# Kernel tuning notes

Hardware: AMD Instinct MI355X
Metric: run time of the kernel (lower is better)

Reference implementation:

```python
import jax, jax.numpy as jnp
import numpy as np

D = 256          # d_model
NPRE = 16; NMLP = 16; NPOST = 16
K = 4            # top_k
P = NPRE * NMLP * NPOST   # 4096 pathways
HMAX = 5 * D     # max mlp expert hidden width (padded storage)
B, S = 8, 256


def _gelu(z):
    return jax.nn.gelu(z, approximate=False)  # torch nn.GELU default = exact erf


def _ln(z, g, b, eps=1e-5):
    mu = z.mean(-1, keepdims=True)
    v = ((z - mu) ** 2).mean(-1, keepdims=True)
    return (z - mu) * jax.lax.rsqrt(v + eps) * g + b


def setup_inputs() -> dict:
    key = jax.random.key(0)
    ks = jax.random.split(key, 8)

    def nrm(k, shape, scale):
        return jax.random.normal(k, shape, dtype=jnp.float32) * scale

    return {
        "x": nrm(ks[0], (B, S, D), 1.0),
        # router MLP (dropout inactive in eval)
        "rw1": nrm(ks[1], (D, 256), D ** -0.5), "rb1": jnp.zeros((256,), jnp.float32),
        "rw2": nrm(ks[2], (256, 128), 256 ** -0.5), "rb2": jnp.zeros((128,), jnp.float32),
        "rw3": nrm(ks[3], (128, P), 128 ** -0.5), "rb3": jnp.zeros((P,), jnp.float32),
        "temp": jnp.ones((1,), jnp.float32),
        # pre experts: Linear + LayerNorm + act
        "pw": nrm(ks[4], (NPRE, D, D), D ** -0.5), "pb": jnp.zeros((NPRE, D), jnp.float32),
        "pg": jnp.ones((NPRE, D), jnp.float32), "pbb": jnp.zeros((NPRE, D), jnp.float32),
        # mlp experts: variable hidden D*(2+i//4), padded to HMAX (unused cols sliced off)
        "mw1": nrm(ks[5], (NMLP, D, HMAX), D ** -0.5), "mb1": jnp.zeros((NMLP, HMAX), jnp.float32),
        "mw2": nrm(ks[6], (NMLP, HMAX, D), HMAX ** -0.5), "mb2": jnp.zeros((NMLP, D), jnp.float32),
        # post experts: Linear + (LayerNorm if even)
        "qw": nrm(ks[7], (NPOST, D, D), D ** -0.5), "qb": jnp.zeros((NPOST, D), jnp.float32),
        "qg": jnp.ones((NPOST, D), jnp.float32), "qbb": jnp.zeros((NPOST, D), jnp.float32),
    }


def reference(x, rw1, rb1, rw2, rb2, rw3, rb3, temp, pw, pb, pg, pbb,
              mw1, mb1, mw2, mb2, qw, qb, qg, qbb):
    Bv, Sv, Dv = x.shape
    N = Bv * Sv
    xt = x.reshape(N, Dv)

    # ---- router ----
    h = _gelu(xt @ rw1 + rb1)
    h = _gelu(h @ rw2 + rb2)
    scores = h @ rw3 + rb3                                  # [N, P]

    # ---- GLBL load-balance loss (softmax without temperature; torch.var unbiased) ----
    freq = jax.nn.softmax(scores, axis=-1).mean(0)          # [P]
    glbl_loss = P * jnp.var(freq, ddof=1)

    # ---- top-k pathway selection ----
    probs = jax.nn.softmax(scores / temp[0], axis=-1)
    top_vals, top_idx = jax.lax.top_k(probs, K)             # [N, K]
    pw_full = jnp.zeros((N, P), x.dtype).at[jnp.arange(N)[:, None], top_idx].set(top_vals)
    pathway_weights = pw_full / (pw_full.sum(-1, keepdims=True) + 1e-8)

    # ---- decompose pathway index -> (pre, mlp, post) ----
    pre_idx = top_idx // (NMLP * NPOST)
    rem = top_idx % (NMLP * NPOST)
    mlp_idx = rem // NPOST
    post_idx = rem % NPOST

    # ---- pre experts: compute all, gather per (token, slot) ----
    acts = [_gelu, jax.nn.relu, jnp.tanh]
    pre_all = jnp.stack(
        [acts[i % 3](_ln(xt @ pw[i] + pb[i], pg[i], pbb[i])) for i in range(NPRE)],
        axis=1)                                              # [N, NPRE, D]
    x_pre = jnp.take_along_axis(pre_all, pre_idx[:, :, None], axis=1)  # [N, K, D]

    # ---- mlp experts (variable hidden width), masked combine ----
    x_mlp = jnp.zeros_like(x_pre)
    for j in range(NMLP):
        hid = Dv * (2 + j // 4)
        a = _gelu if j % 2 == 0 else jax.nn.relu
        mid = a(jnp.einsum('nkd,dh->nkh', x_pre, mw1[j, :, :hid]) + mb1[j, :hid])
        out = jnp.einsum('nkh,hd->nkd', mid, mw2[j, :hid, :]) + mb2[j]
        x_mlp = x_mlp + jnp.where((mlp_idx == j)[:, :, None], out, 0.0)

    # ---- post experts, masked combine ----
    x_post = jnp.zeros_like(x_mlp)
    for q in range(NPOST):
        out = jnp.einsum('nkd,de->nke', x_mlp, qw[q]) + qb[q]
        if q % 2 == 0:
            out = _ln(out, qg[q], qbb[q])
        x_post = x_post + jnp.where((post_idx == q)[:, :, None], out, 0.0)

    # original weights each pathway by its (unnormalized) top value
    output = (x_post * top_vals[:, :, None]).sum(1).reshape(Bv, Sv, Dv)
    return output, glbl_loss, pathway_weights.reshape(Bv, Sv, P)
```

## Files before the change

### kernel.cpp

```cpp
#include <hip/hip_runtime.h>
#include <math.h>

#define DMODEL 256
#define PWAYS  4096
#define TOPK   4
#define HMAX   1280
#define NTOK   2048
#define NPAIR  (NTOK*TOPK)
#define FSLOTS 16
#define MROWS  64
#define YMLP   8
#define CTOT   56

typedef __attribute__((ext_vector_type(8))) short bf16x8;
typedef __attribute__((ext_vector_type(8))) unsigned short u16x8;
typedef __attribute__((ext_vector_type(4))) float f32x4;

#define MFMA_BF16 __builtin_amdgcn_mfma_f32_16x16x32_bf16

__device__ __forceinline__ float gelu_exact(float z) {
    return 0.5f * z * (1.0f + erff(z * 0.70710678118654752440f));
}

__device__ __forceinline__ unsigned short f32_to_bf16_rne(float f) {
    unsigned u = __float_as_uint(f);
    unsigned r = u + 0x7FFFu + ((u >> 16) & 1u);
    return (unsigned short)(r >> 16);
}

__device__ __forceinline__ float bf16_to_f32(unsigned short h) {
    return __uint_as_float((unsigned)h << 16);
}

__device__ __forceinline__ int chunk_base(int e) {
    int g = e >> 2, r = e & 3;
    return 4 * (2 * g + (g * (g - 1)) / 2) + r * (2 + g);
}


__global__ void k_zero2(float* __restrict__ out, float* __restrict__ x_mlp,
                        int* __restrict__ cnts) {
    const int i = blockIdx.x * 256 + threadIdx.x;
    const int stride = gridDim.x * 256;
    for (int j = i; j < NTOK * DMODEL; j += stride) out[j] = 0.0f;
    for (int j = i; j < NPAIR * DMODEL; j += stride) x_mlp[j] = 0.0f;
    if (i < 192) cnts[i] = 0;
}

__global__ void __launch_bounds__(256) k_cvtx(
    const float* __restrict__ src, unsigned short* __restrict__ dh,
    unsigned short* __restrict__ dl) {
    const size_t i = ((size_t)blockIdx.x * 256 + threadIdx.x) * 4;
    const float4 v = *(const float4*)&src[i];
    ushort4 hv, lv;
    hv.x = f32_to_bf16_rne(v.x); lv.x = f32_to_bf16_rne(v.x - bf16_to_f32(hv.x));
    hv.y = f32_to_bf16_rne(v.y); lv.y = f32_to_bf16_rne(v.y - bf16_to_f32(hv.y));
    hv.z = f32_to_bf16_rne(v.z); lv.z = f32_to_bf16_rne(v.z - bf16_to_f32(hv.z));
    hv.w = f32_to_bf16_rne(v.w); lv.w = f32_to_bf16_rne(v.w - bf16_to_f32(hv.w));
    *(ushort4*)&dh[i] = hv;
    *(ushort4*)&dl[i] = lv;
}

__global__ void __launch_bounds__(256) k_pack12(
    const float* __restrict__ rw1, const float* __restrict__ rw2,
    unsigned short* __restrict__ R1P, unsigned short* __restrict__ R2P) {
    const int bx = blockIdx.x;
    const int tid = threadIdx.x;
    const int kq = tid >> 6, lane = tid & 63;
    const int l15 = lane & 15, lhi = lane >> 4;
    const bool is1 = (bx < 16);
    const int nb = is1 ? bx : (bx - 16);
    const int N = is1 ? 256 : 128;
    const float* src = is1 ? rw1 : rw2;
    unsigned short* dst = is1 ? R1P : R2P;
    const int nblk = is1 ? 16 : 8;
    const int pstride = nblk * 8 * 512;
    const int n = nb * 16 + l15;

    for (int k2 = 0; k2 < 2; ++k2) {
        const int kb = kq + k2 * 4;
        const int k0 = kb * 32 + lhi * 8;
        u16x8 hv, lv;
#pragma unroll
        for (int j = 0; j < 8; ++j) {
            const float f = src[(size_t)(k0 + j) * N + n];
            const unsigned short h = f32_to_bf16_rne(f);
            hv[j] = h;
            lv[j] = f32_to_bf16_rne(f - bf16_to_f32(h));
        }
        const size_t o = ((size_t)nb * 8 + kb) * 512 + (size_t)lane * 8;
        *(u16x8*)&dst[o] = hv;
        *(u16x8*)&dst[o + pstride] = lv;
    }
}

__global__ void __launch_bounds__(256, 2) k_h12(
    const unsigned short* __restrict__ xth, const unsigned short* __restrict__ xtl,
    const unsigned short* __restrict__ R1P, const unsigned short* __restrict__ R2P,
    const float* __restrict__ rb1, const float* __restrict__ rb2,
    unsigned short* __restrict__ h2h, unsigned short* __restrict__ h2l) {
    const int n0 = blockIdx.x * 32;
    const int tid = threadIdx.x;
    const int wid = tid >> 6, lane = tid & 63;
    const int l15 = lane & 15, lhi = lane >> 4;

    __shared__ unsigned short ah[32][264];
    __shared__ unsigned short al[32][264];

    for (int t = tid; t < 1024; t += 256) {
        const int row = t >> 5, seg = (t & 31) * 8;
        const size_t g = (size_t)(n0 + row) * DMODEL + seg;
        *(u16x8*)&ah[row][seg] = *(const u16x8*)&xth[g];
        *(u16x8*)&al[row][seg] = *(const u16x8*)&xtl[g];
    }
    __syncthreads();

    {
        f32x4 acc[2][4];
        const f32x4 zf = {0.f, 0.f, 0.f, 0.f};
#pragma unroll
        for (int ms = 0; ms < 2; ++ms)
#pragma unroll
            for (int ns = 0; ns < 4; ++ns) acc[ms][ns] = zf;

#pragma unroll 1
        for (int kb = 0; kb < 8; ++kb) {
            const int ko = kb * 32 + lhi * 8;
            const bf16x8 a_h0 = *(const bf16x8*)&ah[l15][ko];
            const bf16x8 a_h1 = *(const bf16x8*)&ah[16 + l15][ko];
            const bf16x8 a_l0 = *(const bf16x8*)&al[l15][ko];
            const bf16x8 a_l1 = *(const bf16x8*)&al[16 + l15][ko];
#pragma unroll
            for (int ns = 0; ns < 4; ++ns) {
                const size_t bo = ((size_t)(wid * 4 + ns) * 8 + kb) * 512 + (size_t)lane * 8;
                const bf16x8 bh = *(const bf16x8*)&R1P[bo];
                const bf16x8 bl = *(const bf16x8*)&R1P[bo + 65536];
                acc[0][ns] = MFMA_BF16(a_h0, bh, acc[0][ns], 0, 0, 0);
                acc[1][ns] = MFMA_BF16(a_h1, bh, acc[1][ns], 0, 0, 0);
                acc[0][ns] = MFMA_BF16(a_l0, bh, acc[0][ns], 0, 0, 0);
                acc[1][ns] = MFMA_BF16(a_l1, bh, acc[1][ns], 0, 0, 0);
                acc[0][ns] = MFMA_BF16(a_h0, bl, acc[0][ns], 0, 0, 0);
                acc[1][ns] = MFMA_BF16(a_h1, bl, acc[1][ns], 0, 0, 0);
            }
        }
        __syncthreads();

#pragma unroll
        for (int ms = 0; ms < 2; ++ms)
#pragma unroll
            for (int ns = 0; ns < 4; ++ns) {
                const int col = wid * 64 + ns * 16 + l15;
                const float bias = rb1[col];
#pragma unroll
                for (int r = 0; r < 4; ++r) {
                    const int row = ms * 16 + lhi * 4 + r;
                    const float v = gelu_exact(acc[ms][ns][r] + bias);
                    const unsigned short h = f32_to_bf16_rne(v);
                    ah[row][col] = h;
                    al[row][col] = f32_to_bf16_rne(v - bf16_to_f32(h));
                }
            }
        __syncthreads();
    }

    {
        f32x4 acc2[2][2];
        const f32x4 zf = {0.f, 0.f, 0.f, 0.f};
#pragma unroll
        for (int ms = 0; ms < 2; ++ms)
#pragma unroll
            for (int ns = 0; ns < 2; ++ns) acc2[ms][ns] = zf;

#pragma unroll 1
        for (int kb = 0; kb < 8; ++kb) {
            const int ko = kb * 32 + lhi * 8;
            const bf16x8 a_h0 = *(const bf16x8*)&ah[l15][ko];
            const bf16x8 a_h1 = *(const bf16x8*)&ah[16 + l15][ko];
            const bf16x8 a_l0 = *(const bf16x8*)&al[l15][ko];
            const bf16x8 a_l1 = *(const bf16x8*)&al[16 + l15][ko];
#pragma unroll
            for (int ns = 0; ns < 2; ++ns) {
                const int nb = wid * 2 + ns;
                const size_t bo = ((size_t)nb * 8 + kb) * 512 + (size_t)lane * 8;
                const bf16x8 bh = *(const bf16x8*)&R2P[bo];
                const bf16x8 bl = *(const bf16x8*)&R2P[bo + 32768];
                acc2[0][ns] = MFMA_BF16(a_h0, bh, acc2[0][ns], 0, 0, 0);
                acc2[1][ns] = MFMA_BF16(a_h1, bh, acc2[1][ns], 0, 0, 0);
                acc2[0][ns] = MFMA_BF16(a_l0, bh, acc2[0][ns], 0, 0, 0);
                acc2[1][ns] = MFMA_BF16(a_l1, bh, acc2[1][ns], 0, 0, 0);
                acc2[0][ns] = MFMA_BF16(a_h0, bl, acc2[0][ns], 0, 0, 0);
                acc2[1][ns] = MFMA_BF16(a_h1, bl, acc2[1][ns], 0, 0, 0);
            }
        }

#pragma unroll
        for (int ms = 0; ms < 2; ++ms)
#pragma unroll
            for (int ns = 0; ns < 2; ++ns) {
                const int col = wid * 32 + ns * 16 + l15;
                const float bias = rb2[col];
#pragma unroll
                for (int r = 0; r < 4; ++r) {
                    const int row = ms * 16 + lhi * 4 + r;
                    const float v = gelu_exact(acc2[ms][ns][r] + bias);
                    const unsigned short h = f32_to_bf16_rne(v);
                    const size_t o = (size_t)(n0 + row) * 128 + col;
                    h2h[o] = h;
                    h2l[o] = f32_to_bf16_rne(v - bf16_to_f32(h));
                }
            }
    }
}

__global__ void __launch_bounds__(256) k_pack3(
    const float* __restrict__ rw3, unsigned short* __restrict__ P3) {
    const int nb = blockIdx.x;
    const int tid = threadIdx.x;
    const int kb = tid >> 6, lane = tid & 63;
    const int l15 = lane & 15, lhi = lane >> 4;
    const int k0 = kb * 32 + lhi * 8;
    const int n = nb * 16 + l15;
    u16x8 hv, lv;
#pragma unroll
    for (int j = 0; j < 8; ++j) {
        const float f = rw3[(size_t)(k0 + j) * PWAYS + n];
        const unsigned short h = f32_to_bf16_rne(f);
        hv[j] = h;
        lv[j] = f32_to_bf16_rne(f - bf16_to_f32(h));
    }
    const size_t o0 = ((size_t)(0 * 256 + nb) * 4 + kb) * 512 + (size_t)lane * 8;
    const size_t o1 = ((size_t)(1 * 256 + nb) * 4 + kb) * 512 + (size_t)lane * 8;
    *(u16x8*)&P3[o0] = hv;
    *(u16x8*)&P3[o1] = lv;
}

__global__ void __launch_bounds__(256) k_packq(
    const float* __restrict__ pw, const float* __restrict__ qw,
    unsigned short* __restrict__ PPK, unsigned short* __restrict__ QPK) {
    const int e = blockIdx.x;
    const int which = blockIdx.y;
    const int kb = blockIdx.z;
    const int tid = threadIdx.x;
    const int wid = tid >> 6, lane = tid & 63;
    const int l15 = lane & 15, lhi = lane >> 4;
    const float* src = which ? qw : pw;
    unsigned short* dst = which ? QPK : PPK;

    for (int nb = wid; nb < 16; nb += 4) {
        const int n = nb * 16 + l15;
        const int k0 = kb * 32 + lhi * 8;
        u16x8 hv, lv;
#pragma unroll
        for (int j = 0; j < 8; ++j) {
            const float f = src[(size_t)e * DMODEL * DMODEL + (size_t)(k0 + j) * DMODEL + n];
            const unsigned short h = f32_to_bf16_rne(f);
            hv[j] = h;
            lv[j] = f32_to_bf16_rne(f - bf16_to_f32(h));
        }
        const size_t o0 = ((((size_t)e * 2 + 0) * 16 + nb) * 8 + kb) * 512 + (size_t)lane * 8;
        const size_t o1 = ((((size_t)e * 2 + 1) * 16 + nb) * 8 + kb) * 512 + (size_t)lane * 8;
        *(u16x8*)&dst[o0] = hv;
        *(u16x8*)&dst[o1] = lv;
    }
}

__global__ void __launch_bounds__(256, 2) k_scores(
    const unsigned short* __restrict__ h2h, const unsigned short* __restrict__ h2l,
    const unsigned short* __restrict__ P3, const float* __restrict__ rb3,
    float* __restrict__ scores) {
    const int n0 = blockIdx.x * 32;
    const int by = blockIdx.y;
    const int tid = threadIdx.x;
    const int wid = tid >> 6, lane = tid & 63;
    const int l15 = lane & 15, lhi = lane >> 4;

    __shared__ unsigned short ah[32][136];
    __shared__ unsigned short al[32][136];

    for (int t = tid; t < 512; t += 256) {
        const int row = t >> 4, seg = (t & 15) * 8;
        const size_t g = (size_t)(n0 + row) * 128 + seg;
        *(u16x8*)&ah[row][seg] = *(const u16x8*)&h2h[g];
        *(u16x8*)&al[row][seg] = *(const u16x8*)&h2l[g];
    }
    __syncthreads();

    f32x4 acc[2][4];
    const f32x4 zf = {0.f, 0.f, 0.f, 0.f};
#pragma unroll
    for (int ms = 0; ms < 2; ++ms)
#pragma unroll
        for (int ns = 0; ns < 4; ++ns) acc[ms][ns] = zf;

#pragma unroll 1
    for (int kb = 0; kb < 4; ++kb) {
        const int ko = kb * 32 + lhi * 8;
        const bf16x8 a_h0 = *(const bf16x8*)&ah[l15][ko];
        const bf16x8 a_h1 = *(const bf16x8*)&ah[16 + l15][ko];
        const bf16x8 a_l0 = *(const bf16x8*)&al[l15][ko];
        const bf16x8 a_l1 = *(const bf16x8*)&al[16 + l15][ko];
#pragma unroll
        for (int ns = 0; ns < 4; ++ns) {
            const int nb = by * 16 + wid * 4 + ns;
            const size_t bo = ((size_t)nb * 4 + kb) * 512 + (size_t)lane * 8;
            const bf16x8 bh = *(const bf16x8*)&P3[bo];
            const bf16x8 bl = *(const bf16x8*)&P3[bo + 524288];
            acc[0][ns] = MFMA_BF16(a_h0, bh, acc[0][ns], 0, 0, 0);
            acc[1][ns] = MFMA_BF16(a_h1, bh, acc[1][ns], 0, 0, 0);
            acc[0][ns] = MFMA_BF16(a_l0, bh, acc[0][ns], 0, 0, 0);
            acc[1][ns] = MFMA_BF16(a_l1, bh, acc[1][ns], 0, 0, 0);
            acc[0][ns] = MFMA_BF16(a_h0, bl, acc[0][ns], 0, 0, 0);
            acc[1][ns] = MFMA_BF16(a_h1, bl, acc[1][ns], 0, 0, 0);
        }
    }

#pragma unroll
    for (int ms = 0; ms < 2; ++ms)
#pragma unroll
        for (int ns = 0; ns < 4; ++ns) {
            const int col = by * 256 + wid * 64 + ns * 16 + l15;
            const float bias = rb3[col];
#pragma unroll
            for (int r = 0; r < 4; ++r) {
                const int row = n0 + ms * 16 + lhi * 4 + r;
                scores[(size_t)row * PWAYS + col] = acc[ms][ns][r] + bias;
            }
        }
}

__global__ void __launch_bounds__(256) k_topk(
    const float* __restrict__ scores, const float* __restrict__ temp,
    int* __restrict__ top_idx, float* __restrict__ top_vals,
    float* __restrict__ pw_out, float* __restrict__ tok_m, float* __restrict__ tok_i) {
    const int n = blockIdx.x;
    const int tid = threadIdx.x;
    const int wid = tid >> 6, lane = tid & 63;
    const float* row = scores + (size_t)n * PWAYS;

    float sv[16];
#pragma unroll
    for (int i = 0; i < 16; ++i) sv[i] = row[tid + i * 256];

    __shared__ float wred[4];
    __shared__ float wr1[4], wrT[4];
    __shared__ float wbv[4];
    __shared__ int wbi[4];
    __shared__ int sel[TOPK];
    __shared__ float selv[TOPK];
    __shared__ float pwv[TOPK];

    float lmax = -3.402823466e38f;
#pragma unroll
    for (int i = 0; i < 16; ++i) lmax = fmaxf(lmax, sv[i]);
    for (int o = 32; o > 0; o >>= 1) lmax = fmaxf(lmax, __shfl_down(lmax, o));
    if (lane == 0) wred[wid] = lmax;
    __syncthreads();
    const float m = fmaxf(fmaxf(wred[0], wred[1]), fmaxf(wred[2], wred[3]));

    const float invT = 1.0f / temp[0];
    float e1 = 0.f, eT = 0.f;
#pragma unroll
    for (int i = 0; i < 16; ++i) {
        const float d = sv[i] - m;
        e1 += expf(d);
        eT += expf(d * invT);
    }
    for (int o = 32; o > 0; o >>= 1) { e1 += __shfl_down(e1, o); eT += __shfl_down(eT, o); }
    if (lane == 0) { wr1[wid] = e1; wrT[wid] = eT; }
    __syncthreads();
    const float sum1 = wr1[0] + wr1[1] + wr1[2] + wr1[3];
    const float sumT = wrT[0] + wrT[1] + wrT[2] + wrT[3];

    for (int r = 0; r < TOPK; ++r) {
        float bv = -3.402823466e38f;
        int bi = PWAYS;
#pragma unroll
        for (int i = 0; i < 16; ++i) {
            const int p = tid + i * 256;
            bool skip = false;
            for (int u = 0; u < r; ++u) if (sel[u] == p) skip = true;
            if (!skip && sv[i] > bv) { bv = sv[i]; bi = p; }
        }
        for (int o = 32; o > 0; o >>= 1) {
            const float ov = __shfl_down(bv, o);
            const int oi = __shfl_down(bi, o);
            if (ov > bv || (ov == bv && oi < bi)) { bv = ov; bi = oi; }
        }
        if (lane == 0) { wbv[wid] = bv; wbi[wid] = bi; }
        __syncthreads();
        if (tid == 0) {
            float b = wbv[0]; int bidx = wbi[0];
            for (int w = 1; w < 4; ++w)
                if (wbv[w] > b || (wbv[w] == b && wbi[w] < bidx)) { b = wbv[w]; bidx = wbi[w]; }
            sel[r] = bidx; selv[r] = b;
        }
        __syncthreads();
    }

    if (tid == 0) {
        float tv[TOPK];
        float wsum = 1e-8f;
#pragma unroll
        for (int k2 = 0; k2 < TOPK; ++k2) {
            tv[k2] = expf((selv[k2] - m) * invT) / sumT;
            wsum += tv[k2];
        }
        const float invw = 1.0f / wsum;
#pragma unroll
        for (int k2 = 0; k2 < TOPK; ++k2) {
            top_idx[n * TOPK + k2] = sel[k2];
            top_vals[n * TOPK + k2] = tv[k2];
            pwv[k2] = tv[k2] * invw;
        }
        tok_m[n] = m;
        tok_i[n] = 1.0f / sum1;
    }
    __syncthreads();

#pragma unroll
    for (int i = 0; i < 16; ++i) {
        const int p = tid + i * 256;
        float v = 0.0f;
#pragma unroll
        for (int r = 0; r < TOPK; ++r) if (p == sel[r]) v = pwv[r];
        pw_out[(size_t)n * PWAYS + p] = v;
    }
}

__global__ void __launch_bounds__(256) k_freq(
    const float* __restrict__ scores, const float* __restrict__ tok_m,
    const float* __restrict__ tok_i, float* __restrict__ freq_part) {
    const int bx = blockIdx.x;
    const int by = blockIdx.y;
    const int tid = threadIdx.x;
    const int wid = tid >> 6, lane = tid & 63;
    const int col = bx * 64 + lane;

    float acc = 0.f;
    const int r0 = by * 128;
    for (int r = r0 + wid; r < r0 + 128; r += 4) {
        const float mm = tok_m[r], iv = tok_i[r];
        acc += expf(scores[(size_t)r * PWAYS + col] - mm) * iv;
    }
    __shared__ float fs[4][64];
    fs[wid][lane] = acc;
    __syncthreads();
    if (wid == 0)
        freq_part[(size_t)by * PWAYS + col] = fs[0][lane] + fs[1][lane] + fs[2][lane] + fs[3][lane];
}

__global__ void k_freq_loss(const float* __restrict__ freq_part, float* __restrict__ out_loss) {
    __shared__ float fl[PWAYS];
    __shared__ float red[256];
    const int tid = threadIdx.x;
    for (int p = tid; p < PWAYS; p += 256) {
        float s = 0.f;
        for (int sl = 0; sl < FSLOTS; sl++) s += freq_part[(size_t)sl * PWAYS + p];
        fl[p] = s * (1.0f / NTOK);
    }
    __syncthreads();
    float s = 0.f;
    for (int p = tid; p < PWAYS; p += 256) s += fl[p];
    red[tid] = s; __syncthreads();
    for (int st = 128; st > 0; st >>= 1) { if (tid < st) red[tid] += red[tid + st]; __syncthreads(); }
    const float mu = red[0] * (1.0f / PWAYS);
    __syncthreads();
    float ss = 0.f;
    for (int p = tid; p < PWAYS; p += 256) {
        float d = fl[p] - mu;
        ss += d * d;
    }
    red[tid] = ss; __syncthreads();
    for (int st = 128; st > 0; st >>= 1) { if (tid < st) red[tid] += red[tid + st]; __syncthreads(); }
    if (tid == 0)
        out_loss[0] = (float)PWAYS * red[0] / (float)(PWAYS - 1);
}


__global__ void k_count(const int* __restrict__ top_idx, int* __restrict__ counts) {
    const int p = blockIdx.x * 256 + threadIdx.x;
    if (p >= NPAIR) return;
    const int idx = top_idx[p];
    atomicAdd(&counts[0 * 16 + (idx >> 8)], 1);
    atomicAdd(&counts[1 * 16 + ((idx >> 4) & 15)], 1);
    atomicAdd(&counts[2 * 16 + (idx & 15)], 1);
}

__global__ void k_prefix(const int* __restrict__ counts, int* __restrict__ offsets,
                         int* __restrict__ cursors) {
    if (threadIdx.x != 0 || blockIdx.x != 0) return;
    for (int s = 0; s < 3; s++) {
        int run = 0;
        for (int e = 0; e < 16; e++) {
            offsets[s * 16 + e] = run;
            cursors[s * 16 + e] = run;
            run += counts[s * 16 + e];
        }
    }
}

__global__ void k_scatter(const int* __restrict__ top_idx, int* __restrict__ cursors,
                          int* __restrict__ lists) {
    const int p = blockIdx.x * 256 + threadIdx.x;
    if (p >= NPAIR) return;
    const int idx = top_idx[p];
    int pos;
    pos = atomicAdd(&cursors[0 * 16 + (idx >> 8)], 1);        lists[0 * NPAIR + pos] = p;
    pos = atomicAdd(&cursors[1 * 16 + ((idx >> 4) & 15)], 1); lists[1 * NPAIR + pos] = p;
    pos = atomicAdd(&cursors[2 * 16 + (idx & 15)], 1);        lists[2 * NPAIR + pos] = p;
}

__global__ void __launch_bounds__(256) k_packw(
    const float* __restrict__ mw1, const float* __restrict__ mw2,
    unsigned short* __restrict__ W1P, unsigned short* __restrict__ W2P) {
    const int cl = blockIdx.x;
    const int which = blockIdx.y;
    const int kb = blockIdx.z;
    int e = 0;
    while (e < 15 && chunk_base(e + 1) <= cl) ++e;
    const int ch = cl - chunk_base(e);
    const int hbase = ch * 256;
    const int tid = threadIdx.x;
    const int wid = tid >> 6, lane = tid & 63;
    const int l15 = lane & 15, lhi = lane >> 4;

    unsigned short* dst = which ? W2P : W1P;

    for (int nb = wid; nb < 16; nb += 4) {
        const int n = nb * 16 + l15;
        const int k0 = kb * 32 + lhi * 8;
        u16x8 hv, lv;
#pragma unroll
        for (int j = 0; j < 8; ++j) {
            float f;
            if (which == 0)
                f = mw1[((size_t)e * DMODEL + (k0 + j)) * HMAX + hbase + n];
            else
                f = mw2[((size_t)e * HMAX + hbase + k0 + j) * DMODEL + n];
            const unsigned short h = f32_to_bf16_rne(f);
            hv[j] = h;
            lv[j] = f32_to_bf16_rne(f - bf16_to_f32(h));
        }
        const size_t o0 = ((((size_t)cl * 2 + 0) * 16 + nb) * 8 + kb) * 512 + (size_t)lane * 8;
        const size_t o1 = ((((size_t)cl * 2 + 1) * 16 + nb) * 8 + kb) * 512 + (size_t)lane * 8;
        *(u16x8*)&dst[o0] = hv;
        *(u16x8*)&dst[o1] = lv;
    }
}

__global__ void __launch_bounds__(256, 2) k_pre_mfma(
    const unsigned short* __restrict__ xth, const unsigned short* __restrict__ xtl,
    const unsigned short* __restrict__ PPK,
    const float* __restrict__ pb, const float* __restrict__ pg, const float* __restrict__ pbb,
    const int* __restrict__ counts, const int* __restrict__ offsets,
    const int* __restrict__ lists,
    unsigned short* __restrict__ x_h, unsigned short* __restrict__ x_l) {
    const int e = blockIdx.x;
    const int cnt = counts[e];
    if (cnt == 0) return;
    const int off = offsets[e];
    const int am = e % 3;
    const int tid = threadIdx.x;
    const int wid = tid >> 6, lane = tid & 63;
    const int l15 = lane & 15, lhi = lane >> 4;

    __shared__ int prs[32];
    __shared__ unsigned short ah[32][264];
    __shared__ unsigned short al[32][264];
    __shared__ float s1s[4][32], s2s[4][32];
    __shared__ float mus[32], ivs[32];

    float bias4[4], g4[4], bb4[4];
#pragma unroll
    for (int ns = 0; ns < 4; ++ns) {
        const int col = wid * 64 + ns * 16 + l15;
        bias4[ns] = pb[e * DMODEL + col];
        g4[ns] = pg[e * DMODEL + col];
        bb4[ns] = pbb[e * DMODEL + col];
    }
    const size_t wbase = (size_t)e * 2 * 65536;

    for (int base = blockIdx.y * 32; base < cnt; base += 16 * 32) {
        const int Tact = min(32, cnt - base);
        if (tid < 32) prs[tid] = lists[off + base + min(tid, Tact - 1)];
        __syncthreads();
        for (int t = tid; t < 1024; t += 256) {
            const int row = t >> 5, seg = (t & 31) * 8;
            const size_t gsrc = (size_t)(prs[row] >> 2) * DMODEL + seg;
            *(uint4*)&ah[row][seg] = *(const uint4*)&xth[gsrc];
            *(uint4*)&al[row][seg] = *(const uint4*)&xtl[gsrc];
        }
        __syncthreads();

        f32x4 acc[2][4];
        const f32x4 zf = {0.f, 0.f, 0.f, 0.f};
#pragma unroll
        for (int ms = 0; ms < 2; ++ms)
#pragma unroll
            for (int ns = 0; ns < 4; ++ns) acc[ms][ns] = zf;

#pragma unroll 1
        for (int kb = 0; kb < 8; ++kb) {
            const int ko = kb * 32 + lhi * 8;
            const bf16x8 a_h0 = *(const bf16x8*)&ah[l15][ko];
            const bf16x8 a_h1 = *(const bf16x8*)&ah[16 + l15][ko];
            const bf16x8 a_l0 = *(const bf16x8*)&al[l15][ko];
            const bf16x8 a_l1 = *(const bf16x8*)&al[16 + l15][ko];
#pragma unroll
            for (int ns = 0; ns < 4; ++ns) {
                const size_t bo = wbase + (size_t)(((wid * 4 + ns) * 8 + kb) * 512 + lane * 8);
                const bf16x8 bh = *(const bf16x8*)&PPK[bo];
                const bf16x8 bl = *(const bf16x8*)&PPK[bo + 65536];
                acc[0][ns] = MFMA_BF16(a_h0, bh, acc[0][ns], 0, 0, 0);
                acc[1][ns] = MFMA_BF16(a_h1, bh, acc[1][ns], 0, 0, 0);
                acc[0][ns] = MFMA_BF16(a_l0, bh, acc[0][ns], 0, 0, 0);
                acc[1][ns] = MFMA_BF16(a_l1, bh, acc[1][ns], 0, 0, 0);
                acc[0][ns] = MFMA_BF16(a_h0, bl, acc[0][ns], 0, 0, 0);
                acc[1][ns] = MFMA_BF16(a_h1, bl, acc[1][ns], 0, 0, 0);
            }
        }

#pragma unroll
        for (int ms = 0; ms < 2; ++ms)
#pragma unroll
            for (int r = 0; r < 4; ++r) {
                float s1 = 0.f, s2 = 0.f;
#pragma unroll
                for (int ns = 0; ns < 4; ++ns) {
                    const float v = acc[ms][ns][r] + bias4[ns];
                    s1 += v; s2 += v * v;
                }
#pragma unroll
                for (int o = 1; o < 16; o <<= 1) {
                    s1 += __shfl_xor(s1, o);
                    s2 += __shfl_xor(s2, o);
                }
                if (l15 == 0) {
                    s1s[wid][ms * 16 + lhi * 4 + r] = s1;
                    s2s[wid][ms * 16 + lhi * 4 + r] = s2;
                }
            }
        __syncthreads();
        if (tid < 32) {
            const float s1 = s1s[0][tid] + s1s[1][tid] + s1s[2][tid] + s1s[3][tid];
            const float s2 = s2s[0][tid] + s2s[1][tid] + s2s[2][tid] + s2s[3][tid];
            const float mu = s1 * (1.0f / DMODEL);
            mus[tid] = mu;
            ivs[tid] = rsqrtf(s2 * (1.0f / DMODEL) - mu * mu + 1e-5f);
        }
        __syncthreads();

#pragma unroll
        for (int ms = 0; ms < 2; ++ms)
#pragma unroll
            for (int ns = 0; ns < 4; ++ns) {
                const int col = wid * 64 + ns * 16 + l15;
#pragma unroll
                for (int r = 0; r < 4; ++r) {
                    const int row = ms * 16 + lhi * 4 + r;
                    if (row < Tact) {
                        const float v = acc[ms][ns][r] + bias4[ns];
                        float y = (v - mus[row]) * ivs[row] * g4[ns] + bb4[ns];
                        y = (am == 0) ? gelu_exact(y) : (am == 1 ? fmaxf(y, 0.f) : tanhf(y));
                        const unsigned short h = f32_to_bf16_rne(y);
                        const size_t o = (size_t)prs[row] * DMODEL + col;
                        x_h[o] = h;
                        x_l[o] = f32_to_bf16_rne(y - bf16_to_f32(h));
                    }
                }
            }
        __syncthreads();
    }
}

__global__ void __launch_bounds__(256, 2) k_mlp_mfma(
    const unsigned short* __restrict__ x_h, const unsigned short* __restrict__ x_l,
    const unsigned short* __restrict__ W1P, const unsigned short* __restrict__ W2P,
    const float* __restrict__ mb1, const float* __restrict__ mb2,
    const int* __restrict__ counts, const int* __restrict__ offsets,
    const int* __restrict__ lists, float* __restrict__ x_mlp) {
    const int p = blockIdx.x & 7;
    const int j = blockIdx.x >> 3;
    const int ea = p;
    const int eb = (p < 4) ? (p + 12) : (p + 4);
    const int na = (2 + (ea >> 2)) * YMLP;
    int e, ch, y;
    if (j < na) { e = ea; ch = j >> 3; y = j & 7; }
    else        { e = eb; ch = (j - na) >> 3; y = (j - na) & 7; }

    const int cnt = counts[16 + e];
    if (cnt == 0) return;
    const int off = offsets[16 + e];
    const int cl = chunk_base(e) + ch;
    const bool is_gelu = ((e & 1) == 0);
    const int tid = threadIdx.x;
    const int wid = tid >> 6, lane = tid & 63;
    const int l15 = lane & 15, lhi = lane >> 4;

    __shared__ int prs[MROWS];
    __shared__ unsigned short ah[MROWS][264];
    __shared__ unsigned short al[MROWS][264];

    float hb_s[4], ob_s[4];
#pragma unroll
    for (int ns = 0; ns < 4; ++ns) {
        const int col = wid * 64 + ns * 16 + l15;
        hb_s[ns] = mb1[e * HMAX + ch * DMODEL + col];
        ob_s[ns] = (ch == 0) ? mb2[e * DMODEL + col] : 0.0f;
    }

    const size_t wbase = (size_t)cl * 2 * 65536;

    for (int base = y * MROWS; base < cnt; base += YMLP * MROWS) {
        const int Tact = min(MROWS, cnt - base);
        if (tid < MROWS) prs[tid] = lists[NPAIR + off + base + min(tid, Tact - 1)];
        __syncthreads();
        for (int t = tid; t < 2048; t += 256) {
            const int row = t >> 5, seg = (t & 31) * 8;
            const size_t gsrc = (size_t)prs[row] * DMODEL + seg;
            *(uint4*)&ah[row][seg] = *(const uint4*)&x_h[gsrc];
            *(uint4*)&al[row][seg] = *(const uint4*)&x_l[gsrc];
        }
        __syncthreads();

        {
            f32x4 acc[4][4];
            const f32x4 zf = {0.f, 0.f, 0.f, 0.f};
#pragma unroll
            for (int ms = 0; ms < 4; ++ms)
#pragma unroll
                for (int ns = 0; ns < 4; ++ns) acc[ms][ns] = zf;

#pragma unroll 1
            for (int kb = 0; kb < 8; ++kb) {
                const int ko = kb * 32 + lhi * 8;
#pragma unroll
                for (int ns = 0; ns < 4; ++ns) {
                    const size_t bo = wbase + (size_t)(((wid * 4 + ns) * 8 + kb) * 512 + lane * 8);
                    const bf16x8 bh = *(const bf16x8*)&W1P[bo];
                    const bf16x8 bl = *(const bf16x8*)&W1P[bo + 65536];
#pragma unroll
                    for (int ms = 0; ms < 4; ++ms) {
                        const bf16x8 a_h = *(const bf16x8*)&ah[ms * 16 + l15][ko];
                        const bf16x8 a_l = *(const bf16x8*)&al[ms * 16 + l15][ko];
                        acc[ms][ns] = MFMA_BF16(a_h, bh, acc[ms][ns], 0, 0, 0);
                        acc[ms][ns] = MFMA_BF16(a_l, bh, acc[ms][ns], 0, 0, 0);
                        acc[ms][ns] = MFMA_BF16(a_h, bl, acc[ms][ns], 0, 0, 0);
                    }
                }
            }
            __syncthreads();

#pragma unroll
            for (int ms = 0; ms < 4; ++ms)
#pragma unroll
                for (int ns = 0; ns < 4; ++ns) {
                    const int col = wid * 64 + ns * 16 + l15;
#pragma unroll
                    for (int r = 0; r < 4; ++r) {
                        const int row = ms * 16 + lhi * 4 + r;
                        float v = acc[ms][ns][r] + hb_s[ns];
                        v = is_gelu ? gelu_exact(v) : fmaxf(v, 0.0f);
                        const unsigned short h = f32_to_bf16_rne(v);
                        ah[row][col] = h;
                        al[row][col] = f32_to_bf16_rne(v - bf16_to_f32(h));
                    }
                }
            __syncthreads();
        }

        {
            f32x4 acc2[4][4];
            const f32x4 zf = {0.f, 0.f, 0.f, 0.f};
#pragma unroll
            for (int ms = 0; ms < 4; ++ms)
#pragma unroll
                for (int ns = 0; ns < 4; ++ns) acc2[ms][ns] = zf;

#pragma unroll 1
            for (int kb = 0; kb < 8; ++kb) {
                const int ko = kb * 32 + lhi * 8;
#pragma unroll
                for (int ns = 0; ns < 4; ++ns) {
                    const size_t bo = wbase + (size_t)(((wid * 4 + ns) * 8 + kb) * 512 + lane * 8);
                    const bf16x8 bh = *(const bf16x8*)&W2P[bo];
                    const bf16x8 bl = *(const bf16x8*)&W2P[bo + 65536];
#pragma unroll
                    for (int ms = 0; ms < 4; ++ms) {
                        const bf16x8 a_h = *(const bf16x8*)&ah[ms * 16 + l15][ko];
                        const bf16x8 a_l = *(const bf16x8*)&al[ms * 16 + l15][ko];
                        acc2[ms][ns] = MFMA_BF16(a_h, bh, acc2[ms][ns], 0, 0, 0);
                        acc2[ms][ns] = MFMA_BF16(a_l, bh, acc2[ms][ns], 0, 0, 0);
                        acc2[ms][ns] = MFMA_BF16(a_h, bl, acc2[ms][ns], 0, 0, 0);
                    }
                }
            }

#pragma unroll
            for (int ms = 0; ms < 4; ++ms)
#pragma unroll
                for (int ns = 0; ns < 4; ++ns) {
                    const int col = wid * 64 + ns * 16 + l15;
#pragma unroll
                    for (int r = 0; r < 4; ++r) {
                        const int row = ms * 16 + lhi * 4 + r;
                        if (row < Tact)
                            atomicAdd(&x_mlp[(size_t)prs[row] * DMODEL + col],
                                      acc2[ms][ns][r] + ob_s[ns]);
                    }
                }
        }
        __syncthreads();
    }
}

__global__ void __launch_bounds__(256, 2) k_post_mfma(
    const float* __restrict__ x_mlp,
    const unsigned short* __restrict__ QPK,
    const float* __restrict__ qb, const float* __restrict__ qg, const float* __restrict__ qbb,
    const float* __restrict__ top_val,
    const int* __restrict__ counts, const int* __restrict__ offsets,
    const int* __restrict__ lists, float* __restrict__ out) {
    const int e = blockIdx.x;
    const int cnt = counts[32 + e];
    if (cnt == 0) return;
    const int off = offsets[32 + e];
    const bool has_ln = ((e & 1) == 0);
    const int tid = threadIdx.x;
    const int wid = tid >> 6, lane = tid & 63;
    const int l15 = lane & 15, lhi = lane >> 4;

    __shared__ int prs[32];
    __shared__ float tvs[32];
    __shared__ unsigned short ah[32][264];
    __shared__ unsigned short al[32][264];
    __shared__ float s1s[4][32], s2s[4][32];
    __shared__ float mus[32], ivs[32];

    float bias4[4], g4[4], bb4[4];
#pragma unroll
    for (int ns = 0; ns < 4; ++ns) {
        const int col = wid * 64 + ns * 16 + l15;
        bias4[ns] = qb[e * DMODEL + col];
        g4[ns] = qg[e * DMODEL + col];
        bb4[ns] = qbb[e * DMODEL + col];
    }
    const size_t wbase = (size_t)e * 2 * 65536;

    for (int base = blockIdx.y * 32; base < cnt; base += 16 * 32) {
        const int Tact = min(32, cnt - base);
        if (tid < 32) {
            const int p = lists[2 * NPAIR + off + base + min(tid, Tact - 1)];
            prs[tid] = p;
            tvs[tid] = top_val[p];
        }
        __syncthreads();
        for (int t = tid; t < 1024; t += 256) {
            const int row = t >> 5, seg = (t & 31) * 8;
            const float* src = &x_mlp[(size_t)prs[row] * DMODEL + seg];
            const float4 v0 = *(const float4*)&src[0];
            const float4 v1 = *(const float4*)&src[4];
            u16x8 hv, lv;
            const float fv[8] = {v0.x, v0.y, v0.z, v0.w, v1.x, v1.y, v1.z, v1.w};
#pragma unroll
            for (int jj = 0; jj < 8; ++jj) {
                const unsigned short h = f32_to_bf16_rne(fv[jj]);
                hv[jj] = h;
                lv[jj] = f32_to_bf16_rne(fv[jj] - bf16_to_f32(h));
            }
            *(u16x8*)&ah[row][seg] = hv;
            *(u16x8*)&al[row][seg] = lv;
        }
        __syncthreads();

        f32x4 acc[2][4];
        const f32x4 zf = {0.f, 0.f, 0.f, 0.f};
#pragma unroll
        for (int ms = 0; ms < 2; ++ms)
#pragma unroll
            for (int ns = 0; ns < 4; ++ns) acc[ms][ns] = zf;

#pragma unroll 1
        for (int kb = 0; kb < 8; ++kb) {
            const int ko = kb * 32 + lhi * 8;
            const bf16x8 a_h0 = *(const bf16x8*)&ah[l15][ko];
            const bf16x8 a_h1 = *(const bf16x8*)&ah[16 + l15][ko];
            const bf16x8 a_l0 = *(const bf16x8*)&al[l15][ko];
            const bf16x8 a_l1 = *(const bf16x8*)&al[16 + l15][ko];
#pragma unroll
            for (int ns = 0; ns < 4; ++ns) {
                const size_t bo = wbase + (size_t)(((wid * 4 + ns) * 8 + kb) * 512 + lane * 8);
                const bf16x8 bh = *(const bf16x8*)&QPK[bo];
                const bf16x8 bl = *(const bf16x8*)&QPK[bo + 65536];
                acc[0][ns] = MFMA_BF16(a_h0, bh, acc[0][ns], 0, 0, 0);
                acc[1][ns] = MFMA_BF16(a_h1, bh, acc[1][ns], 0, 0, 0);
                acc[0][ns] = MFMA_BF16(a_l0, bh, acc[0][ns], 0, 0, 0);
                acc[1][ns] = MFMA_BF16(a_l1, bh, acc[1][ns], 0, 0, 0);
                acc[0][ns] = MFMA_BF16(a_h0, bl, acc[0][ns], 0, 0, 0);
                acc[1][ns] = MFMA_BF16(a_h1, bl, acc[1][ns], 0, 0, 0);
            }
        }

        if (has_ln) {
#pragma unroll
            for (int ms = 0; ms < 2; ++ms)
#pragma unroll
                for (int r = 0; r < 4; ++r) {
                    float s1 = 0.f, s2 = 0.f;
#pragma unroll
                    for (int ns = 0; ns < 4; ++ns) {
                        const float v = acc[ms][ns][r] + bias4[ns];
                        s1 += v; s2 += v * v;
                    }
#pragma unroll
                    for (int o = 1; o < 16; o <<= 1) {
                        s1 += __shfl_xor(s1, o);
                        s2 += __shfl_xor(s2, o);
                    }
                    if (l15 == 0) {
                        s1s[wid][ms * 16 + lhi * 4 + r] = s1;
                        s2s[wid][ms * 16 + lhi * 4 + r] = s2;
                    }
                }
            __syncthreads();
            if (tid < 32) {
                const float s1 = s1s[0][tid] + s1s[1][tid] + s1s[2][tid] + s1s[3][tid];
                const float s2 = s2s[0][tid] + s2s[1][tid] + s2s[2][tid] + s2s[3][tid];
                const float mu = s1 * (1.0f / DMODEL);
                mus[tid] = mu;
                ivs[tid] = rsqrtf(s2 * (1.0f / DMODEL) - mu * mu + 1e-5f);
            }
            __syncthreads();
        }

#pragma unroll
        for (int ms = 0; ms < 2; ++ms)
#pragma unroll
            for (int ns = 0; ns < 4; ++ns) {
                const int col = wid * 64 + ns * 16 + l15;
#pragma unroll
                for (int r = 0; r < 4; ++r) {
                    const int row = ms * 16 + lhi * 4 + r;
                    if (row < Tact) {
                        const float v = acc[ms][ns][r] + bias4[ns];
                        const float t = has_ln ? ((v - mus[row]) * ivs[row] * g4[ns] + bb4[ns]) : v;
                        atomicAdd(&out[(size_t)(prs[row] >> 2) * DMODEL + col], tvs[row] * t);
                    }
                }
            }
        __syncthreads();
    }
}

extern "C" void kernel_launch(void* const* d_in, const int* in_sizes, int n_in,
                              void* d_out, int out_size, void* d_ws, size_t ws_size,
                              hipStream_t stream) {
    (void)in_sizes; (void)n_in; (void)out_size; (void)ws_size;

    const float* x    = (const float*)d_in[0];
    const float* rw1  = (const float*)d_in[1];
    const float* rb1  = (const float*)d_in[2];
    const float* rw2  = (const float*)d_in[3];
    const float* rb2  = (const float*)d_in[4];
    const float* rw3  = (const float*)d_in[5];
    const float* rb3  = (const float*)d_in[6];
    const float* temp = (const float*)d_in[7];
    const float* pw   = (const float*)d_in[8];
    const float* pb   = (const float*)d_in[9];
    const float* pg   = (const float*)d_in[10];
    const float* pbb  = (const float*)d_in[11];
    const float* mw1  = (const float*)d_in[12];
    const float* mb1  = (const float*)d_in[13];
    const float* mw2  = (const float*)d_in[14];
    const float* mb2  = (const float*)d_in[15];
    const float* qw   = (const float*)d_in[16];
    const float* qb   = (const float*)d_in[17];
    const float* qg   = (const float*)d_in[18];
    const float* qbb  = (const float*)d_in[19];

    float* out      = (float*)d_out;
    float* out_loss = out + (size_t)NTOK * DMODEL;
    float* out_pw   = out_loss + 1;

    float* freq_part = (float*)d_ws;
    int*   top_idx   = (int*)(freq_part + (size_t)FSLOTS * PWAYS);
    float* top_val   = (float*)(top_idx + NPAIR);
    int*   counts    = (int*)(top_val + NPAIR);
    int*   offsets   = counts + 64;
    int*   cursors   = offsets + 64;
    int*   lists     = cursors + 64;
    float* x_mlp     = (float*)(lists + 3 * NPAIR);
    unsigned short* x_h = (unsigned short*)(x_mlp + (size_t)NPAIR * DMODEL);
    unsigned short* x_l = x_h + (size_t)NPAIR * DMODEL;
    unsigned short* W1P = x_l + (size_t)NPAIR * DMODEL;
    unsigned short* W2P = W1P + (size_t)CTOT * 2 * 65536;
    unsigned short* P3  = W2P + (size_t)CTOT * 2 * 65536;
    unsigned short* h2h = P3 + 2 * 524288;
    unsigned short* h2l = h2h + (size_t)NTOK * 128;
    float* tok_m = (float*)(h2l + (size_t)NTOK * 128);
    float* tok_i = tok_m + NTOK;
    unsigned short* xth = (unsigned short*)(tok_i + NTOK);
    unsigned short* xtl = xth + (size_t)NTOK * DMODEL;
    unsigned short* PPK = xtl + (size_t)NTOK * DMODEL;
    unsigned short* QPK = PPK + (size_t)16 * 2 * 65536;
    unsigned short* R1P = QPK + (size_t)16 * 2 * 65536;
    unsigned short* R2P = R1P + 2 * 65536;
    float* scores = x_mlp;

    k_cvtx<<<NTOK * DMODEL / 1024, 256, 0, stream>>>(x, xth, xtl);
    k_pack12<<<24, 256, 0, stream>>>(rw1, rw2, R1P, R2P);
    k_pack3<<<256, 256, 0, stream>>>(rw3, P3);
    k_packq<<<dim3(16, 2, 8), 256, 0, stream>>>(pw, qw, PPK, QPK);
    k_h12<<<NTOK / 32, 256, 0, stream>>>(xth, xtl, R1P, R2P, rb1, rb2, h2h, h2l);
    k_scores<<<dim3(64, 16), 256, 0, stream>>>(h2h, h2l, P3, rb3, scores);
    k_topk<<<NTOK, 256, 0, stream>>>(scores, temp, top_idx, top_val, out_pw, tok_m, tok_i);
    k_freq<<<dim3(64, 16), 256, 0, stream>>>(scores, tok_m, tok_i, freq_part);
    k_freq_loss<<<1, 256, 0, stream>>>(freq_part, out_loss);

    k_zero2<<<1024, 256, 0, stream>>>(out, x_mlp, counts);
    k_count<<<NPAIR / 256, 256, 0, stream>>>(top_idx, counts);
    k_prefix<<<1, 64, 0, stream>>>(counts, offsets, cursors);
    k_scatter<<<NPAIR / 256, 256, 0, stream>>>(top_idx, cursors, lists);
    k_packw<<<dim3(CTOT, 2, 8), 256, 0, stream>>>(mw1, mw2, W1P, W2P);
    k_pre_mfma<<<dim3(16, 16), 256, 0, stream>>>(xth, xtl, PPK, pb, pg, pbb,
                                                 counts, offsets, lists, x_h, x_l);
    k_mlp_mfma<<<CTOT * YMLP, 256, 0, stream>>>(x_h, x_l, W1P, W2P, mb1, mb2,
                                                counts, offsets, lists, x_mlp);
    k_post_mfma<<<dim3(16, 16), 256, 0, stream>>>(x_mlp, QPK, qb, qg, qbb, top_val,
                                                  counts, offsets, lists, out);
}
```

Baseline: 501.1 us.

## Merge packing kernels and fold expert counting and prefix into top-k

Merges the x conversion and the rw1/rw2/rw3/pw/qw bf16 hi/lo packing into a single k_pack_front launch, which also zeroes the counters. Expert counting moves into k_topk via atomics, and a last-block-done pattern computes the offsets and cursors there, which removes the separate count and prefix kernels. The goal is fewer kernel launches and fewer inter-kernel gaps. The cost is heavier atomic traffic and a threadfence inside top-k, and k_scores is relaunched as a 1-D grid.

```diff
diff --git a/kernel.cpp b/kernel.cpp
--- a/kernel.cpp
+++ b/kernel.cpp
@@ -37,477 +37,99 @@
     return 4 * (2 * g + (g * (g - 1)) / 2) + r * (2 + g);
 }
 
-
-__global__ void k_zero2(float* __restrict__ out, float* __restrict__ x_mlp,
-                        int* __restrict__ cnts) {
-    const int i = blockIdx.x * 256 + threadIdx.x;
-    const int stride = gridDim.x * 256;
-    for (int j = i; j < NTOK * DMODEL; j += stride) out[j] = 0.0f;
-    for (int j = i; j < NPAIR * DMODEL; j += stride) x_mlp[j] = 0.0f;
-    if (i < 192) cnts[i] = 0;
-}
-
-__global__ void __launch_bounds__(256) k_cvtx(
-    const float* __restrict__ src, unsigned short* __restrict__ dh,
-    unsigned short* __restrict__ dl) {
-    const size_t i = ((size_t)blockIdx.x * 256 + threadIdx.x) * 4;
-    const float4 v = *(const float4*)&src[i];
-    ushort4 hv, lv;
-    hv.x = f32_to_bf16_rne(v.x); lv.x = f32_to_bf16_rne(v.x - bf16_to_f32(hv.x));
-    hv.y = f32_to_bf16_rne(v.y); lv.y = f32_to_bf16_rne(v.y - bf16_to_f32(hv.y));
-    hv.z = f32_to_bf16_rne(v.z); lv.z = f32_to_bf16_rne(v.z - bf16_to_f32(hv.z));
-    hv.w = f32_to_bf16_rne(v.w); lv.w = f32_to_bf16_rne(v.w - bf16_to_f32(hv.w));
-    *(ushort4*)&dh[i] = hv;
-    *(ushort4*)&dl[i] = lv;
-}
-
-__global__ void __launch_bounds__(256) k_pack12(
+__global__ void __launch_bounds__(256) k_pack_front(
+    const float* __restrict__ x,
     const float* __restrict__ rw1, const float* __restrict__ rw2,
-    unsigned short* __restrict__ R1P, unsigned short* __restrict__ R2P) {
-    const int bx = blockIdx.x;
+    const float* __restrict__ rw3,
+    const float* __restrict__ pw, const float* __restrict__ qw,
+    unsigned short* __restrict__ xth, unsigned short* __restrict__ xtl,
+    unsigned short* __restrict__ R1P, unsigned short* __restrict__ R2P,
+    unsigned short* __restrict__ P3,
+    unsigned short* __restrict__ PPK, unsigned short* __restrict__ QPK,
+    int* __restrict__ cnts) {
+    const int wg = blockIdx.x;
     const int tid = threadIdx.x;
-    const int kq = tid >> 6, lane = tid & 63;
+    const int lane = tid & 63;
     const int l15 = lane & 15, lhi = lane >> 4;
-    const bool is1 = (bx < 16);
-    const int nb = is1 ? bx : (bx - 16);
-    const int N = is1 ? 256 : 128;
-    const float* src = is1 ? rw1 : rw2;
-    unsigned short* dst = is1 ? R1P : R2P;
-    const int nblk = is1 ? 16 : 8;
-    const int pstride = nblk * 8 * 512;
-    const int n = nb * 16 + l15;
-
-    for (int k2 = 0; k2 < 2; ++k2) {
-        const int kb = kq + k2 * 4;
+
+    if (wg < 512) {
+        const size_t i = ((size_t)wg * 256 + tid) * 4;
+        const float4 v = *(const float4*)&x[i];
+        ushort4 hv, lv;
+        hv.x = f32_to_bf16_rne(v.x); lv.x = f32_to_bf16_rne(v.x - bf16_to_f32(hv.x));
+        hv.y = f32_to_bf16_rne(v.y); lv.y = f32_to_bf16_rne(v.y - bf16_to_f32(hv.y));
+        hv.z = f32_to_bf16_rne(v.z); lv.z = f32_to_bf16_rne(v.z - bf16_to_f32(hv.z));
+        hv.w = f32_to_bf16_rne(v.w); lv.w = f32_to_bf16_rne(v.w - bf16_to_f32(hv.w));
+        *(ushort4*)&xth[i] = hv;
+        *(ushort4*)&xtl[i] = lv;
+    } else if (wg < 536) {
+        const int bx = wg - 512;
+        const int kq = tid >> 6;
+        const bool is1 = (bx < 16);
+        const int nb = is1 ? bx : (bx - 16);
+        const int N = is1 ? 256 : 128;
+        const float* src = is1 ? rw1 : rw2;
+        unsigned short* dst = is1 ? R1P : R2P;
+        const int nblk = is1 ? 16 : 8;
+        const int pstride = nblk * 8 * 512;
+        const int n = nb * 16 + l15;
+        for (int k2 = 0; k2 < 2; ++k2) {
+            const int kb = kq + k2 * 4;
+            const int k0 = kb * 32 + lhi * 8;
+            u16x8 hv, lv;
+#pragma unroll
+            for (int j = 0; j < 8; ++j) {
+                const float f = src[(size_t)(k0 + j) * N + n];
+                const unsigned short h = f32_to_bf16_rne(f);
+                hv[j] = h;
+                lv[j] = f32_to_bf16_rne(f - bf16_to_f32(h));
+            }
+            const size_t o = ((size_t)nb * 8 + kb) * 512 + (size_t)lane * 8;
+            *(u16x8*)&dst[o] = hv;
+            *(u16x8*)&dst[o + pstride] = lv;
+        }
+    } else if (wg < 792) {
+        const int nb = wg - 536;
+        const int kb = tid >> 6;
         const int k0 = kb * 32 + lhi * 8;
+        const int n = nb * 16 + l15;
         u16x8 hv, lv;
 #pragma unroll
         for (int j = 0; j < 8; ++j) {
-            const float f = src[(size_t)(k0 + j) * N + n];
+            const float f = rw3[(size_t)(k0 + j) * PWAYS + n];
             const unsigned short h = f32_to_bf16_rne(f);
             hv[j] = h;
             lv[j] = f32_to_bf16_rne(f - bf16_to_f32(h));
         }
-        const size_t o = ((size_t)nb * 8 + kb) * 512 + (size_t)lane * 8;
-        *(u16x8*)&dst[o] = hv;
-        *(u16x8*)&dst[o + pstride] = lv;
-    }
-}
-
-__global__ void __launch_bounds__(256, 2) k_h12(
-    const unsigned short* __restrict__ xth, const unsigned short* __restrict__ xtl,
-    const unsigned short* __restrict__ R1P, const unsigned short* __restrict__ R2P,
-    const float* __restrict__ rb1, const float* __restrict__ rb2,
-    unsigned short* __restrict__ h2h, unsigned short* __restrict__ h2l) {
-    const int n0 = blockIdx.x * 32;
-    const int tid = threadIdx.x;
-    const int wid = tid >> 6, lane = tid & 63;
-    const int l15 = lane & 15, lhi = lane >> 4;
-
-    __shared__ unsigned short ah[32][264];
-    __shared__ unsigned short al[32][264];
-
-    for (int t = tid; t < 1024; t += 256) {
-        const int row = t >> 5, seg = (t & 31) * 8;
-        const size_t g = (size_t)(n0 + row) * DMODEL + seg;
-        *(u16x8*)&ah[row][seg] = *(const u16x8*)&xth[g];
-        *(u16x8*)&al[row][seg] = *(const u16x8*)&xtl[g];
-    }
-    __syncthreads();
-
-    {
-        f32x4 acc[2][4];
-        const f32x4 zf = {0.f, 0.f, 0.f, 0.f};
-#pragma unroll
-        for (int ms = 0; ms < 2; ++ms)
-#pragma unroll
-            for (int ns = 0; ns < 4; ++ns) acc[ms][ns] = zf;
-
-#pragma unroll 1
-        for (int kb = 0; kb < 8; ++kb) {
-            const int ko = kb * 32 + lhi * 8;
-            const bf16x8 a_h0 = *(const bf16x8*)&ah[l15][ko];
-            const bf16x8 a_h1 = *(const bf16x8*)&ah[16 + l15][ko];
-            const bf16x8 a_l0 = *(const bf16x8*)&al[l15][ko];
-            const bf16x8 a_l1 = *(const bf16x8*)&al[16 + l15][ko];
-#pragma unroll
-            for (int ns = 0; ns < 4; ++ns) {
-                const size_t bo = ((size_t)(wid * 4 + ns) * 8 + kb) * 512 + (size_t)lane * 8;
-                const bf16x8 bh = *(const bf16x8*)&R1P[bo];
-                const bf16x8 bl = *(const bf16x8*)&R1P[bo + 65536];
-                acc[0][ns] = MFMA_BF16(a_h0, bh, acc[0][ns], 0, 0, 0);
-                acc[1][ns] = MFMA_BF16(a_h1, bh, acc[1][ns], 0, 0, 0);
-                acc[0][ns] = MFMA_BF16(a_l0, bh, acc[0][ns], 0, 0, 0);
-                acc[1][ns] = MFMA_BF16(a_l1, bh, acc[1][ns], 0, 0, 0);
-                acc[0][ns] = MFMA_BF16(a_h0, bl, acc[0][ns], 0, 0, 0);
-                acc[1][ns] = MFMA_BF16(a_h1, bl, acc[1][ns], 0, 0, 0);
-            }
-        }
-        __syncthreads();
-
-#pragma unroll
-        for (int ms = 0; ms < 2; ++ms)
-#pragma unroll
-            for (int ns = 0; ns < 4; ++ns) {
-                const int col = wid * 64 + ns * 16 + l15;
-                const float bias = rb1[col];
-#pragma unroll
-                for (int r = 0; r < 4; ++r) {
-                    const int row = ms * 16 + lhi * 4 + r;
-                    const float v = gelu_exact(acc[ms][ns][r] + bias);
-                    const unsigned short h = f32_to_bf16_rne(v);
-                    ah[row][col] = h;
-                    al[row][col] = f32_to_bf16_rne(v - bf16_to_f32(h));
-                }
-            }
-        __syncthreads();
-    }
-
-    {
-        f32x4 acc2[2][2];
-        const f32x4 zf = {0.f, 0.f, 0.f, 0.f};
-#pragma unroll
-        for (int ms = 0; ms < 2; ++ms)
-#pragma unroll
-            for (int ns = 0; ns < 2; ++ns) acc2[ms][ns] = zf;
-
-#pragma unroll 1
-        for (int kb = 0; kb < 8; ++kb) {
-            const int ko = kb * 32 + lhi * 8;
-            const bf16x8 a_h0 = *(const bf16x8*)&ah[l15][ko];
-            const bf16x8 a_h1 = *(const bf16x8*)&ah[16 + l15][ko];
-            const bf16x8 a_l0 = *(const bf16x8*)&al[l15][ko];
-            const bf16x8 a_l1 = *(const bf16x8*)&al[16 + l15][ko];
-#pragma unroll
-            for (int ns = 0; ns < 2; ++ns) {
-                const int nb = wid * 2 + ns;
-                const size_t bo = ((size_t)nb * 8 + kb) * 512 + (size_t)lane * 8;
-                const bf16x8 bh = *(const bf16x8*)&R2P[bo];
-                const bf16x8 bl = *(const bf16x8*)&R2P[bo + 32768];
-                acc2[0][ns] = MFMA_BF16(a_h0, bh, acc2[0][ns], 0, 0, 0);
-                acc2[1][ns] = MFMA_BF16(a_h1, bh, acc2[1][ns], 0, 0, 0);
-                acc2[0][ns] = MFMA_BF16(a_l0, bh, acc2[0][ns], 0, 0, 0);
-                acc2[1][ns] = MFMA_BF16(a_l1, bh, acc2[1][ns], 0, 0, 0);
-                acc2[0][ns] = MFMA_BF16(a_h0, bl, acc2[0][ns], 0, 0, 0);
-                acc2[1][ns] = MFMA_BF16(a_h1, bl, acc2[1][ns], 0, 0, 0);
-            }
-        }
-
-#pragma unroll
-        for (int ms = 0; ms < 2; ++ms)
-#pragma unroll
-            for (int ns = 0; ns < 2; ++ns) {
-                const int col = wid * 32 + ns * 16 + l15;
-                const float bias = rb2[col];
-#pragma unroll
-                for (int r = 0; r < 4; ++r) {
-                    const int row = ms * 16 + lhi * 4 + r;
-                    const float v = gelu_exact(acc2[ms][ns][r] + bias);
-                    const unsigned short h = f32_to_bf16_rne(v);
-                    const size_t o = (size_t)(n0 + row) * 128 + col;
-                    h2h[o] = h;
-                    h2l[o] = f32_to_bf16_rne(v - bf16_to_f32(h));
-                }
-            }
-    }
-}
-
-__global__ void __launch_bounds__(256) k_pack3(
-    const float* __restrict__ rw3, unsigned short* __restrict__ P3) {
-    const int nb = blockIdx.x;
-    const int tid = threadIdx.x;
-    const int kb = tid >> 6, lane = tid & 63;
-    const int l15 = lane & 15, lhi = lane >> 4;
-    const int k0 = kb * 32 + lhi * 8;
-    const int n = nb * 16 + l15;
-    u16x8 hv, lv;
-#pragma unroll
-    for (int j = 0; j < 8; ++j) {
-        const float f = rw3[(size_t)(k0 + j) * PWAYS + n];
-        const unsigned short h = f32_to_bf16_rne(f);
-        hv[j] = h;
-        lv[j] = f32_to_bf16_rne(f - bf16_to_f32(h));
-    }
-    const size_t o0 = ((size_t)(0 * 256 + nb) * 4 + kb) * 512 + (size_t)lane * 8;
-    const size_t o1 = ((size_t)(1 * 256 + nb) * 4 + kb) * 512 + (size_t)lane * 8;
-    *(u16x8*)&P3[o0] = hv;
-    *(u16x8*)&P3[o1] = lv;
-}
-
-__global__ void __launch_bounds__(256) k_packq(
-    const float* __restrict__ pw, const float* __restrict__ qw,
-    unsigned short* __restrict__ PPK, unsigned short* __restrict__ QPK) {
-    const int e = blockIdx.x;
-    const int which = blockIdx.y;
-    const int kb = blockIdx.z;
-    const int tid = threadIdx.x;
-    const int wid = tid >> 6, lane = tid & 63;
-    const int l15 = lane & 15, lhi = lane >> 4;
-    const float* src = which ? qw : pw;
-    unsigned short* dst = which ? QPK : PPK;
-
-    for (int nb = wid; nb < 16; nb += 4) {
-        const int n = nb * 16 + l15;
-        const int k0 = kb * 32 + lhi * 8;
-        u16x8 hv, lv;
-#pragma unroll
-        for (int j = 0; j < 8; ++j) {
-            const float f = src[(size_t)e * DMODEL * DMODEL + (size_t)(k0 + j) * DMODEL + n];
-            const unsigned short h = f32_to_bf16_rne(f);
-            hv[j] = h;
-            lv[j] = f32_to_bf16_rne(f - bf16_to_f32(h));
-        }
-        const size_t o0 = ((((size_t)e * 2 + 0) * 16 + nb) * 8 + kb) * 512 + (size_t)lane * 8;
-        const size_t o1 = ((((size_t)e * 2 + 1) * 16 + nb) * 8 + kb) * 512 + (size_t)lane * 8;
-        *(u16x8*)&dst[o0] = hv;
-        *(u16x8*)&dst[o1] = lv;
-    }
-}
-
-__global__ void __launch_bounds__(256, 2) k_scores(
-    const unsigned short* __restrict__ h2h, const unsigned short* __restrict__ h2l,
-    const unsigned short* __restrict__ P3, const float* __restrict__ rb3,
-    float* __restrict__ scores) {
-    const int n0 = blockIdx.x * 32;
-    const int by = blockIdx.y;
-    const int tid = threadIdx.x;
-    const int wid = tid >> 6, lane = tid & 63;
-    const int l15 = lane & 15, lhi = lane >> 4;
-
-    __shared__ unsigned short ah[32][136];
-    __shared__ unsigned short al[32][136];
-
-    for (int t = tid; t < 512; t += 256) {
-        const int row = t >> 4, seg = (t & 15) * 8;
-        const size_t g = (size_t)(n0 + row) * 128 + seg;
-        *(u16x8*)&ah[row][seg] = *(const u16x8*)&h2h[g];
-        *(u16x8*)&al[row][seg] = *(const u16x8*)&h2l[g];
-    }
-    __syncthreads();
-
-    f32x4 acc[2][4];
-    const f32x4 zf = {0.f, 0.f, 0.f, 0.f};
-#pragma unroll
-    for (int ms = 0; ms < 2; ++ms)
-#pragma unroll
-        for (int ns = 0; ns < 4; ++ns) acc[ms][ns] = zf;
-
-#pragma unroll 1
-    for (int kb = 0; kb < 4; ++kb) {
-        const int ko = kb * 32 + lhi * 8;
-        const bf16x8 a_h0 = *(const bf16x8*)&ah[l15][ko];
-        const bf16x8 a_h1 = *(const bf16x8*)&ah[16 + l15][ko];
-        const bf16x8 a_l0 = *(const bf16x8*)&al[l15][ko];
-        const bf16x8 a_l1 = *(const bf16x8*)&al[16 + l15][ko];
-#pragma unroll
-        for (int ns = 0; ns < 4; ++ns) {
-            const int nb = by * 16 + wid * 4 + ns;
-            const size_t bo = ((size_t)nb * 4 + kb) * 512 + (size_t)lane * 8;
-            const bf16x8 bh = *(const bf16x8*)&P3[bo];
-            const bf16x8 bl = *(const bf16x8*)&P3[bo + 524288];
-            acc[0][ns] = MFMA_BF16(a_h0, bh, acc[0][ns], 0, 0, 0);
-            acc[1][ns] = MFMA_BF16(a_h1, bh, acc[1][ns], 0, 0, 0);
-            acc[0][ns] = MFMA_BF16(a_l0, bh, acc[0][ns], 0, 0, 0);
-            acc[1][ns] = MFMA_BF16(a_l1, bh, acc[1][ns], 0, 0, 0);
-            acc[0][ns] = MFMA_BF16(a_h0, bl, acc[0][ns], 0, 0, 0);
-            acc[1][ns] = MFMA_BF16(a_h1, bl, acc[1][ns], 0, 0, 0);
-        }
-    }
-
-#pragma unroll
-    for (int ms = 0; ms < 2; ++ms)
-#pragma unroll
-        for (int ns = 0; ns < 4; ++ns) {
-            const int col = by * 256 + wid * 64 + ns * 16 + l15;
-            const float bias = rb3[col];
-#pragma unroll
-            for (int r = 0; r < 4; ++r) {
-                const int row = n0 + ms * 16 + lhi * 4 + r;
-                scores[(size_t)row * PWAYS + col] = acc[ms][ns][r] + bias;
-            }
-        }
-}
-
-__global__ void __launch_bounds__(256) k_topk(
-    const float* __restrict__ scores, const float* __restrict__ temp,
-    int* __restrict__ top_idx, float* __restrict__ top_vals,
-    float* __restrict__ pw_out, float* __restrict__ tok_m, float* __restrict__ tok_i) {
-    const int n = blockIdx.x;
-    const int tid = threadIdx.x;
-    const int wid = tid >> 6, lane = tid & 63;
-    const float* row = scores + (size_t)n * PWAYS;
-
-    float sv[16];
-#pragma unroll
-    for (int i = 0; i < 16; ++i) sv[i] = row[tid + i * 256];
-
-    __shared__ float wred[4];
-    __shared__ float wr1[4], wrT[4];
-    __shared__ float wbv[4];
-    __shared__ int wbi[4];
-    __shared__ int sel[TOPK];
-    __shared__ float selv[TOPK];
-    __shared__ float pwv[TOPK];
-
-    float lmax = -3.402823466e38f;
-#pragma unroll
-    for (int i = 0; i < 16; ++i) lmax = fmaxf(lmax, sv[i]);
-    for (int o = 32; o > 0; o >>= 1) lmax = fmaxf(lmax, __shfl_down(lmax, o));
-    if (lane == 0) wred[wid] = lmax;
-    __syncthreads();
-    const float m = fmaxf(fmaxf(wred[0], wred[1]), fmaxf(wred[2], wred[3]));
-
-    const float invT = 1.0f / temp[0];
-    float e1 = 0.f, eT = 0.f;
-#pragma unroll
-    for (int i = 0; i < 16; ++i) {
-        const float d = sv[i] - m;
-        e1 += expf(d);
-        eT += expf(d * invT);
-    }
-    for (int o = 32; o > 0; o >>= 1) { e1 += __shfl_down(e1, o); eT += __shfl_down(eT, o); }
-    if (lane == 0) { wr1[wid] = e1; wrT[wid] = eT; }
-    __syncthreads();
-    const float sum1 = wr1[0] + wr1[1] + wr1[2] + wr1[3];
-    const float sumT = wrT[0] + wrT[1] + wrT[2] + wrT[3];
-
-    for (int r = 0; r < TOPK; ++r) {
-        float bv = -3.402823466e38f;
-        int bi = PWAYS;
-#pragma unroll
-        for (int i = 0; i < 16; ++i) {
-            const int p = tid + i * 256;
-            bool skip = false;
-            for (int u = 0; u < r; ++u) if (sel[u] == p) skip = true;
-            if (!skip && sv[i] > bv) { bv = sv[i]; bi = p; }
-        }
-        for (int o = 32; o > 0; o >>= 1) {
-            const float ov = __shfl_down(bv, o);
-            const int oi = __shfl_down(bi, o);
-            if (ov > bv || (ov == bv && oi < bi)) { bv = ov; bi = oi; }
-        }
-        if (lane == 0) { wbv[wid] = bv; wbi[wid] = bi; }
-        __syncthreads();
-        if (tid == 0) {
-            float b = wbv[0]; int bidx = wbi[0];
-            for (int w = 1; w < 4; ++w)
-                if (wbv[w] > b || (wbv[w] == b && wbi[w] < bidx)) { b = wbv[w]; bidx = wbi[w]; }
-            sel[r] = bidx; selv[r] = b;
-        }
-        __syncthreads();
-    }
-
-    if (tid == 0) {
-        float tv[TOPK];
-        float wsum = 1e-8f;
-#pragma unroll
-        for (int k2 = 0; k2 < TOPK; ++k2) {
-            tv[k2] = expf((selv[k2] - m) * invT) / sumT;
-            wsum += tv[k2];
-        }
-        const float invw = 1.0f / wsum;
-#pragma unroll
-        for (int k2 = 0; k2 < TOPK; ++k2) {
-            top_idx[n * TOPK + k2] = sel[k2];
-            top_vals[n * TOPK + k2] = tv[k2];
-            pwv[k2] = tv[k2] * invw;
-        }
-        tok_m[n] = m;
-        tok_i[n] = 1.0f / sum1;
-    }
-    __syncthreads();
-
-#pragma unroll
-    for (int i = 0; i < 16; ++i) {
-        const int p = tid + i * 256;
-        float v = 0.0f;
-#pragma unroll
-        for (int r = 0; r < TOPK; ++r) if (p == sel[r]) v = pwv[r];
-        pw_out[(size_t)n * PWAYS + p] = v;
-    }
-}
-
-__global__ void __launch_bounds__(256) k_freq(
-    const float* __restrict__ scores, const float* __restrict__ tok_m,
-    const float* __restrict__ tok_i, float* __restrict__ freq_part) {
-    const int bx = blockIdx.x;
-    const int by = blockIdx.y;
-    const int tid = threadIdx.x;
-    const int wid = tid >> 6, lane = tid & 63;
-    const int col = bx * 64 + lane;
-
-    float acc = 0.f;
-    const int r0 = by * 128;
-    for (int r = r0 + wid; r < r0 + 128; r += 4) {
-        const float mm = tok_m[r], iv = tok_i[r];
-        acc += expf(scores[(size_t)r * PWAYS + col] - mm) * iv;
-    }
-    __shared__ float fs[4][64];
-    fs[wid][lane] = acc;
-    __syncthreads();
-    if (wid == 0)
-        freq_part[(size_t)by * PWAYS + col] = fs[0][lane] + fs[1][lane] + fs[2][lane] + fs[3][lane];
-}
-
-__global__ void k_freq_loss(const float* __restrict__ freq_part, float* __restrict__ out_loss) {
-    __shared__ float fl[PWAYS];
-    __shared__ float red[256];
-    const int tid = threadIdx.x;
-    for (int p = tid; p < PWAYS; p += 256) {
-        float s = 0.f;
-        for (int sl = 0; sl < FSLOTS; sl++) s += freq_part[(size_t)sl * PWAYS + p];
-        fl[p] = s * (1.0f / NTOK);
-    }
-    __syncthreads();
-    float s = 0.f;
-    for (int p = tid; p < PWAYS; p += 256) s += fl[p];
-    red[tid] = s; __syncthreads();
-    for (int st = 128; st > 0; st >>= 1) { if (tid < st) red[tid] += red[tid + st]; __syncthreads(); }
-    const float mu = red[0] * (1.0f / PWAYS);
-    __syncthreads();
-    float ss = 0.f;
-    for (int p = tid; p < PWAYS; p += 256) {
-        float d = fl[p] - mu;
-        ss += d * d;
-    }
-    red[tid] = ss; __syncthreads();
-    for (int st = 128; st > 0; st >>= 1) { if (tid < st) red[tid] += red[tid + st]; __syncthreads(); }
-    if (tid == 0)
-        out_loss[0] = (float)PWAYS * red[0] / (float)(PWAYS - 1);
-}
-
-
-__global__ void k_count(const int* __restrict__ top_idx, int* __restrict__ counts) {
-    const int p = blockIdx.x * 256 + threadIdx.x;
-    if (p >= NPAIR) return;
-    const int idx = top_idx[p];
-    atomicAdd(&counts[0 * 16 + (idx >> 8)], 1);
-    atomicAdd(&counts[1 * 16 + ((idx >> 4) & 15)], 1);
-    atomicAdd(&counts[2 * 16 + (idx & 15)], 1);
-}
-
-__global__ void k_prefix(const int* __restrict__ counts, int* __restrict__ offsets,
-                         int* __restrict__ cursors) {
-    if (threadIdx.x != 0 || blockIdx.x != 0) return;
-    for (int s = 0; s < 3; s++) {
-        int run = 0;
-        for (int e = 0; e < 16; e++) {
-            offsets[s * 16 + e] = run;
-            cursors[s * 16 + e] = run;
-            run += counts[s * 16 + e];
-        }
-    }
-}
-
-__global__ void k_scatter(const int* __restrict__ top_idx, int* __restrict__ cursors,
-                          int* __restrict__ lists) {
-    const int p = blockIdx.x * 256 + threadIdx.x;
-    if (p >= NPAIR) return;
-    const int idx = top_idx[p];
-    int pos;
-    pos = atomicAdd(&cursors[0 * 16 + (idx >> 8)], 1);        lists[0 * NPAIR + pos] = p;
-    pos = atomicAdd(&cursors[1 * 16 + ((idx >> 4) & 15)], 1); lists[1 * NPAIR + pos] = p;
-    pos = atomicAdd(&cursors[2 * 16 + (idx & 15)], 1);        lists[2 * NPAIR + pos] = p;
+        const size_t o0 = ((size_t)(0 * 256 + nb) * 4 + kb) * 512 + (size_t)lane * 8;
+        const size_t o1 = ((size_t)(1 * 256 + nb) * 4 + kb) * 512 + (size_t)lane * 8;
+        *(u16x8*)&P3[o0] = hv;
+        *(u16x8*)&P3[o1] = lv;
+    } else if (wg < 1048) {
+        const int idx = wg - 792;
+        const int e = idx & 15, which = (idx >> 4) & 1, kb = idx >> 5;
+        const int wid = tid >> 6;
+        const float* src = which ? qw : pw;
+        unsigned short* dst = which ? QPK : PPK;
+        for (int nb = wid; nb < 16; nb += 4) {
+            const int n = nb * 16 + l15;
+            const int k0 = kb * 32 + lhi * 8;
+            u16x8 hv, lv;
+#pragma unroll
+            for (int j = 0; j < 8; ++j) {
+                const float f = src[(size_t)e * DMODEL * DMODEL + (size_t)(k0 + j) * DMODEL + n];
+                const unsigned short h = f32_to_bf16_rne(f);
+                hv[j] = h;
+                lv[j] = f32_to_bf16_rne(f - bf16_to_f32(h));
+            }
+            const size_t o0 = ((((size_t)e * 2 + 0) * 16 + nb) * 8 + kb) * 512 + (size_t)lane * 8;
+            const size_t o1 = ((((size_t)e * 2 + 1) * 16 + nb) * 8 + kb) * 512 + (size_t)lane * 8;
+            *(u16x8*)&dst[o0] = hv;
+            *(u16x8*)&dst[o1] = lv;
+        }
+    } else {
+        if (tid < 192) cnts[tid] = 0;
+    }
 }
 
 __global__ void __launch_bounds__(256) k_packw(
@@ -546,6 +168,387 @@
         *(u16x8*)&dst[o0] = hv;
         *(u16x8*)&dst[o1] = lv;
     }
+}
+
+
+__global__ void k_zero2(float* __restrict__ out, float* __restrict__ x_mlp) {
+    const int i = blockIdx.x * 256 + threadIdx.x;
+    const int stride = gridDim.x * 256;
+    for (int j = i; j < NTOK * DMODEL; j += stride) out[j] = 0.0f;
+    for (int j = i; j < NPAIR * DMODEL; j += stride) x_mlp[j] = 0.0f;
+}
+
+__global__ void __launch_bounds__(256, 2) k_h12(
+    const unsigned short* __restrict__ xth, const unsigned short* __restrict__ xtl,
+    const unsigned short* __restrict__ R1P, const unsigned short* __restrict__ R2P,
+    const float* __restrict__ rb1, const float* __restrict__ rb2,
+    unsigned short* __restrict__ h2h, unsigned short* __restrict__ h2l) {
+    const int n0 = blockIdx.x * 32;
+    const int tid = threadIdx.x;
+    const int wid = tid >> 6, lane = tid & 63;
+    const int l15 = lane & 15, lhi = lane >> 4;
+
+    __shared__ unsigned short ah[32][264];
+    __shared__ unsigned short al[32][264];
+
+    for (int t = tid; t < 1024; t += 256) {
+        const int row = t >> 5, seg = (t & 31) * 8;
+        const size_t g = (size_t)(n0 + row) * DMODEL + seg;
+        *(u16x8*)&ah[row][seg] = *(const u16x8*)&xth[g];
+        *(u16x8*)&al[row][seg] = *(const u16x8*)&xtl[g];
+    }
+    __syncthreads();
+
+    {
+        f32x4 acc[2][4];
+        const f32x4 zf = {0.f, 0.f, 0.f, 0.f};
+#pragma unroll
+        for (int ms = 0; ms < 2; ++ms)
+#pragma unroll
+            for (int ns = 0; ns < 4; ++ns) acc[ms][ns] = zf;
+
+#pragma unroll 1
+        for (int kb = 0; kb < 8; ++kb) {
+            const int ko = kb * 32 + lhi * 8;
+            const bf16x8 a_h0 = *(const bf16x8*)&ah[l15][ko];
+            const bf16x8 a_h1 = *(const bf16x8*)&ah[16 + l15][ko];
+            const bf16x8 a_l0 = *(const bf16x8*)&al[l15][ko];
+            const bf16x8 a_l1 = *(const bf16x8*)&al[16 + l15][ko];
+#pragma unroll
+            for (int ns = 0; ns < 4; ++ns) {
+                const size_t bo = ((size_t)(wid * 4 + ns) * 8 + kb) * 512 + (size_t)lane * 8;
+                const bf16x8 bh = *(const bf16x8*)&R1P[bo];
+                const bf16x8 bl = *(const bf16x8*)&R1P[bo + 65536];
+                acc[0][ns] = MFMA_BF16(a_h0, bh, acc[0][ns], 0, 0, 0);
+                acc[1][ns] = MFMA_BF16(a_h1, bh, acc[1][ns], 0, 0, 0);
+                acc[0][ns] = MFMA_BF16(a_l0, bh, acc[0][ns], 0, 0, 0);
+                acc[1][ns] = MFMA_BF16(a_l1, bh, acc[1][ns], 0, 0, 0);
+                acc[0][ns] = MFMA_BF16(a_h0, bl, acc[0][ns], 0, 0, 0);
+                acc[1][ns] = MFMA_BF16(a_h1, bl, acc[1][ns], 0, 0, 0);
+            }
+        }
+        __syncthreads();
+
+#pragma unroll
+        for (int ms = 0; ms < 2; ++ms)
+#pragma unroll
+            for (int ns = 0; ns < 4; ++ns) {
+                const int col = wid * 64 + ns * 16 + l15;
+                const float bias = rb1[col];
+#pragma unroll
+                for (int r = 0; r < 4; ++r) {
+                    const int row = ms * 16 + lhi * 4 + r;
+                    const float v = gelu_exact(acc[ms][ns][r] + bias);
+                    const unsigned short h = f32_to_bf16_rne(v);
+                    ah[row][col] = h;
+                    al[row][col] = f32_to_bf16_rne(v - bf16_to_f32(h));
+                }
+            }
+        __syncthreads();
+    }
+
+    {
+        f32x4 acc2[2][2];
+        const f32x4 zf = {0.f, 0.f, 0.f, 0.f};
+#pragma unroll
+        for (int ms = 0; ms < 2; ++ms)
+#pragma unroll
+            for (int ns = 0; ns < 2; ++ns) acc2[ms][ns] = zf;
+
+#pragma unroll 1
+        for (int kb = 0; kb < 8; ++kb) {
+            const int ko = kb * 32 + lhi * 8;
+            const bf16x8 a_h0 = *(const bf16x8*)&ah[l15][ko];
+            const bf16x8 a_h1 = *(const bf16x8*)&ah[16 + l15][ko];
+            const bf16x8 a_l0 = *(const bf16x8*)&al[l15][ko];
+            const bf16x8 a_l1 = *(const bf16x8*)&al[16 + l15][ko];
+#pragma unroll
+            for (int ns = 0; ns < 2; ++ns) {
+                const int nb = wid * 2 + ns;
+                const size_t bo = ((size_t)nb * 8 + kb) * 512 + (size_t)lane * 8;
+                const bf16x8 bh = *(const bf16x8*)&R2P[bo];
+                const bf16x8 bl = *(const bf16x8*)&R2P[bo + 32768];
+                acc2[0][ns] = MFMA_BF16(a_h0, bh, acc2[0][ns], 0, 0, 0);
+                acc2[1][ns] = MFMA_BF16(a_h1, bh, acc2[1][ns], 0, 0, 0);
+                acc2[0][ns] = MFMA_BF16(a_l0, bh, acc2[0][ns], 0, 0, 0);
+                acc2[1][ns] = MFMA_BF16(a_l1, bh, acc2[1][ns], 0, 0, 0);
+                acc2[0][ns] = MFMA_BF16(a_h0, bl, acc2[0][ns], 0, 0, 0);
+                acc2[1][ns] = MFMA_BF16(a_h1, bl, acc2[1][ns], 0, 0, 0);
+            }
+        }
+
+#pragma unroll
+        for (int ms = 0; ms < 2; ++ms)
+#pragma unroll
+            for (int ns = 0; ns < 2; ++ns) {
+                const int col = wid * 32 + ns * 16 + l15;
+                const float bias = rb2[col];
+#pragma unroll
+                for (int r = 0; r < 4; ++r) {
+                    const int row = ms * 16 + lhi * 4 + r;
+                    const float v = gelu_exact(acc2[ms][ns][r] + bias);
+                    const unsigned short h = f32_to_bf16_rne(v);
+                    const size_t o = (size_t)(n0 + row) * 128 + col;
+                    h2h[o] = h;
+                    h2l[o] = f32_to_bf16_rne(v - bf16_to_f32(h));
+                }
+            }
+    }
+}
+
+__global__ void __launch_bounds__(256, 2) k_scores(
+    const unsigned short* __restrict__ h2h, const unsigned short* __restrict__ h2l,
+    const unsigned short* __restrict__ P3, const float* __restrict__ rb3,
+    float* __restrict__ scores) {
+    const int wg = blockIdx.x;
+    const int by = wg & 15;
+    const int n0 = (wg >> 4) * 32;
+    const int tid = threadIdx.x;
+    const int wid = tid >> 6, lane = tid & 63;
+    const int l15 = lane & 15, lhi = lane >> 4;
+
+    __shared__ unsigned short ah[32][136];
+    __shared__ unsigned short al[32][136];
+
+    for (int t = tid; t < 512; t += 256) {
+        const int row = t >> 4, seg = (t & 15) * 8;
+        const size_t g = (size_t)(n0 + row) * 128 + seg;
+        *(u16x8*)&ah[row][seg] = *(const u16x8*)&h2h[g];
+        *(u16x8*)&al[row][seg] = *(const u16x8*)&h2l[g];
+    }
+    __syncthreads();
+
+    f32x4 acc[2][4];
+    const f32x4 zf = {0.f, 0.f, 0.f, 0.f};
+#pragma unroll
+    for (int ms = 0; ms < 2; ++ms)
+#pragma unroll
+        for (int ns = 0; ns < 4; ++ns) acc[ms][ns] = zf;
+
+#pragma unroll 1
+    for (int kb = 0; kb < 4; ++kb) {
+        const int ko = kb * 32 + lhi * 8;
+        const bf16x8 a_h0 = *(const bf16x8*)&ah[l15][ko];
+        const bf16x8 a_h1 = *(const bf16x8*)&ah[16 + l15][ko];
+        const bf16x8 a_l0 = *(const bf16x8*)&al[l15][ko];
+        const bf16x8 a_l1 = *(const bf16x8*)&al[16 + l15][ko];
+#pragma unroll
+        for (int ns = 0; ns < 4; ++ns) {
+            const int nb = by * 16 + wid * 4 + ns;
+            const size_t bo = ((size_t)nb * 4 + kb) * 512 + (size_t)lane * 8;
+            const bf16x8 bh = *(const bf16x8*)&P3[bo];
+            const bf16x8 bl = *(const bf16x8*)&P3[bo + 524288];
+            acc[0][ns] = MFMA_BF16(a_h0, bh, acc[0][ns], 0, 0, 0);
+            acc[1][ns] = MFMA_BF16(a_h1, bh, acc[1][ns], 0, 0, 0);
+            acc[0][ns] = MFMA_BF16(a_l0, bh, acc[0][ns], 0, 0, 0);
+            acc[1][ns] = MFMA_BF16(a_l1, bh, acc[1][ns], 0, 0, 0);
+            acc[0][ns] = MFMA_BF16(a_h0, bl, acc[0][ns], 0, 0, 0);
+            acc[1][ns] = MFMA_BF16(a_h1, bl, acc[1][ns], 0, 0, 0);
+        }
+    }
+
+#pragma unroll
+    for (int ms = 0; ms < 2; ++ms)
+#pragma unroll
+        for (int ns = 0; ns < 4; ++ns) {
+            const int col = by * 256 + wid * 64 + ns * 16 + l15;
+            const float bias = rb3[col];
+#pragma unroll
+            for (int r = 0; r < 4; ++r) {
+                const int row = n0 + ms * 16 + lhi * 4 + r;
+                scores[(size_t)row * PWAYS + col] = acc[ms][ns][r] + bias;
+            }
+        }
+}
+
+__global__ void __launch_bounds__(256) k_topk(
+    const float* __restrict__ scores, const float* __restrict__ temp,
+    int* __restrict__ top_idx, float* __restrict__ top_vals,
+    float* __restrict__ pw_out, float* __restrict__ tok_m, float* __restrict__ tok_i,
+    int* __restrict__ counts, int* __restrict__ offsets, int* __restrict__ cursors) {
+    const int n = blockIdx.x;
+    const int tid = threadIdx.x;
+    const int wid = tid >> 6, lane = tid & 63;
+    const float* row = scores + (size_t)n * PWAYS;
+
+    float sv[16];
+#pragma unroll
+    for (int i = 0; i < 16; ++i) sv[i] = row[tid + i * 256];
+
+    __shared__ float wred[4];
+    __shared__ float wr1[4], wrT[4];
+    __shared__ float wbv[4];
+    __shared__ int wbi[4];
+    __shared__ int sel[TOPK];
+    __shared__ float selv[TOPK];
+    __shared__ float pwv[TOPK];
+    __shared__ int lastflag;
+    __shared__ int cshared[48];
+
+    float lmax = -3.402823466e38f;
+#pragma unroll
+    for (int i = 0; i < 16; ++i) lmax = fmaxf(lmax, sv[i]);
+    for (int o = 32; o > 0; o >>= 1) lmax = fmaxf(lmax, __shfl_down(lmax, o));
+    if (lane == 0) wred[wid] = lmax;
+    __syncthreads();
+    const float m = fmaxf(fmaxf(wred[0], wred[1]), fmaxf(wred[2], wred[3]));
+
+    const float invT = 1.0f / temp[0];
+    float e1 = 0.f, eT = 0.f;
+#pragma unroll
+    for (int i = 0; i < 16; ++i) {
+        const float d = sv[i] - m;
+        e1 += expf(d);
+        eT += expf(d * invT);
+    }
+    for (int o = 32; o > 0; o >>= 1) { e1 += __shfl_down(e1, o); eT += __shfl_down(eT, o); }
+    if (lane == 0) { wr1[wid] = e1; wrT[wid] = eT; }
+    __syncthreads();
+    const float sum1 = wr1[0] + wr1[1] + wr1[2] + wr1[3];
+    const float sumT = wrT[0] + wrT[1] + wrT[2] + wrT[3];
+
+    for (int r = 0; r < TOPK; ++r) {
+        float bv = -3.402823466e38f;
+        int bi = PWAYS;
+#pragma unroll
+        for (int i = 0; i < 16; ++i) {
+            const int p = tid + i * 256;
+            bool skip = false;
+            for (int u = 0; u < r; ++u) if (sel[u] == p) skip = true;
+            if (!skip && sv[i] > bv) { bv = sv[i]; bi = p; }
+        }
+        for (int o = 32; o > 0; o >>= 1) {
+            const float ov = __shfl_down(bv, o);
+            const int oi = __shfl_down(bi, o);
+            if (ov > bv || (ov == bv && oi < bi)) { bv = ov; bi = oi; }
+        }
+        if (lane == 0) { wbv[wid] = bv; wbi[wid] = bi; }
+        __syncthreads();
+        if (tid == 0) {
+            float b = wbv[0]; int bidx = wbi[0];
+            for (int w = 1; w < 4; ++w)
+                if (wbv[w] > b || (wbv[w] == b && wbi[w] < bidx)) { b = wbv[w]; bidx = wbi[w]; }
+            sel[r] = bidx; selv[r] = b;
+        }
+        __syncthreads();
+    }
+
+    if (tid == 0) {
+        float tv[TOPK];
+        float wsum = 1e-8f;
+#pragma unroll
+        for (int k2 = 0; k2 < TOPK; ++k2) {
+            tv[k2] = expf((selv[k2] - m) * invT) / sumT;
+            wsum += tv[k2];
+        }
+        const float invw = 1.0f / wsum;
+#pragma unroll
+        for (int k2 = 0; k2 < TOPK; ++k2) {
+            top_idx[n * TOPK + k2] = sel[k2];
+            top_vals[n * TOPK + k2] = tv[k2];
+            pwv[k2] = tv[k2] * invw;
+        }
+        tok_m[n] = m;
+        tok_i[n] = 1.0f / sum1;
+#pragma unroll
+        for (int r = 0; r < TOPK; ++r) {
+            const int idx = sel[r];
+            atomicAdd(&counts[0 * 16 + (idx >> 8)], 1);
+            atomicAdd(&counts[1 * 16 + ((idx >> 4) & 15)], 1);
+            atomicAdd(&counts[2 * 16 + (idx & 15)], 1);
+        }
+    }
+    __syncthreads();
+
+#pragma unroll
+    for (int i = 0; i < 16; ++i) {
+        const int p = tid + i * 256;
+        float v = 0.0f;
+#pragma unroll
+        for (int r = 0; r < TOPK; ++r) if (p == sel[r]) v = pwv[r];
+        pw_out[(size_t)n * PWAYS + p] = v;
+    }
+
+    if (tid == 0) {
+        __threadfence();
+        lastflag = (atomicAdd(&counts[48], 1) == NTOK - 1);
+    }
+    __syncthreads();
+    if (lastflag) {
+        if (tid < 48) cshared[tid] = atomicAdd(&counts[tid], 0);
+        __syncthreads();
+        if (tid == 0) {
+            for (int s = 0; s < 3; ++s) {
+                int run = 0;
+                for (int e2 = 0; e2 < 16; ++e2) {
+                    offsets[s * 16 + e2] = run;
+                    cursors[s * 16 + e2] = run;
+                    run += cshared[s * 16 + e2];
+                }
+            }
+        }
+    }
+}
+
+__global__ void __launch_bounds__(256) k_freq(
+    const float* __restrict__ scores, const float* __restrict__ tok_m,
+    const float* __restrict__ tok_i, float* __restrict__ freq_part) {
+    const int bx = blockIdx.x;
+    const int by = blockIdx.y;
+    const int tid = threadIdx.x;
+    const int wid = tid >> 6, lane = tid & 63;
+    const int col = bx * 64 + lane;
+
+    float acc = 0.f;
+    const int r0 = by * 128;
+    for (int r = r0 + wid; r < r0 + 128; r += 4) {
+        const float mm = tok_m[r], iv = tok_i[r];
+        acc += expf(scores[(size_t)r * PWAYS + col] - mm) * iv;
+    }
+    __shared__ float fs[4][64];
+    fs[wid][lane] = acc;
+    __syncthreads();
+    if (wid == 0)
+        freq_part[(size_t)by * PWAYS + col] = fs[0][lane] + fs[1][lane] + fs[2][lane] + fs[3][lane];
+}
+
+__global__ void k_freq_loss(const float* __restrict__ freq_part, float* __restrict__ out_loss) {
+    __shared__ float fl[PWAYS];
+    __shared__ float red[256];
+    const int tid = threadIdx.x;
+    for (int p = tid; p < PWAYS; p += 256) {
+        float s = 0.f;
+        for (int sl = 0; sl < FSLOTS; sl++) s += freq_part[(size_t)sl * PWAYS + p];
+        fl[p] = s * (1.0f / NTOK);
+    }
+    __syncthreads();
+    float s = 0.f;
+    for (int p = tid; p < PWAYS; p += 256) s += fl[p];
+    red[tid] = s; __syncthreads();
+    for (int st = 128; st > 0; st >>= 1) { if (tid < st) red[tid] += red[tid + st]; __syncthreads(); }
+    const float mu = red[0] * (1.0f / PWAYS);
+    __syncthreads();
+    float ss = 0.f;
+    for (int p = tid; p < PWAYS; p += 256) {
+        float d = fl[p] - mu;
+        ss += d * d;
+    }
+    red[tid] = ss; __syncthreads();
+    for (int st = 128; st > 0; st >>= 1) { if (tid < st) red[tid] += red[tid + st]; __syncthreads(); }
+    if (tid == 0)
+        out_loss[0] = (float)PWAYS * red[0] / (float)(PWAYS - 1);
+}
+
+
+__global__ void k_scatter(const int* __restrict__ top_idx, int* __restrict__ cursors,
+                          int* __restrict__ lists) {
+    const int p = blockIdx.x * 256 + threadIdx.x;
+    if (p >= NPAIR) return;
+    const int idx = top_idx[p];
+    int pos;
+    pos = atomicAdd(&cursors[0 * 16 + (idx >> 8)], 1);        lists[0 * NPAIR + pos] = p;
+    pos = atomicAdd(&cursors[1 * 16 + ((idx >> 4) & 15)], 1); lists[1 * NPAIR + pos] = p;
+    pos = atomicAdd(&cursors[2 * 16 + (idx & 15)], 1);        lists[2 * NPAIR + pos] = p;
 }
 
 __global__ void __launch_bounds__(256, 2) k_pre_mfma(
@@ -1007,21 +1010,19 @@
     unsigned short* R2P = R1P + 2 * 65536;
     float* scores = x_mlp;
 
-    k_cvtx<<<NTOK * DMODEL / 1024, 256, 0, stream>>>(x, xth, xtl);
-    k_pack12<<<24, 256, 0, stream>>>(rw1, rw2, R1P, R2P);
-    k_pack3<<<256, 256, 0, stream>>>(rw3, P3);
-    k_packq<<<dim3(16, 2, 8), 256, 0, stream>>>(pw, qw, PPK, QPK);
+    k_pack_front<<<1049, 256, 0, stream>>>(x, rw1, rw2, rw3, pw, qw,
+                                           xth, xtl, R1P, R2P, P3, PPK, QPK,
+                                           counts);
     k_h12<<<NTOK / 32, 256, 0, stream>>>(xth, xtl, R1P, R2P, rb1, rb2, h2h, h2l);
-    k_scores<<<dim3(64, 16), 256, 0, stream>>>(h2h, h2l, P3, rb3, scores);
-    k_topk<<<NTOK, 256, 0, stream>>>(scores, temp, top_idx, top_val, out_pw, tok_m, tok_i);
+    k_scores<<<1024, 256, 0, stream>>>(h2h, h2l, P3, rb3, scores);
+    k_topk<<<NTOK, 256, 0, stream>>>(scores, temp, top_idx, top_val, out_pw,
+                                     tok_m, tok_i, counts, offsets, cursors);
     k_freq<<<dim3(64, 16), 256, 0, stream>>>(scores, tok_m, tok_i, freq_part);
     k_freq_loss<<<1, 256, 0, stream>>>(freq_part, out_loss);
 
-    k_zero2<<<1024, 256, 0, stream>>>(out, x_mlp, counts);
-    k_count<<<NPAIR / 256, 256, 0, stream>>>(top_idx, counts);
-    k_prefix<<<1, 64, 0, stream>>>(counts, offsets, cursors);
+    k_zero2<<<1024, 256, 0, stream>>>(out, x_mlp);
+    k_packw<<<dim3(CTOT, 2, 8), 256, 0, stream>>>(mw1, mw2, W1P, W2P);
     k_scatter<<<NPAIR / 256, 256, 0, stream>>>(top_idx, cursors, lists);
-    k_packw<<<dim3(CTOT, 2, 8), 256, 0, stream>>>(mw1, mw2, W1P, W2P);
     k_pre_mfma<<<dim3(16, 16), 256, 0, stream>>>(xth, xtl, PPK, pb, pg, pbb,
                                                  counts, offsets, lists, x_h, x_l);
     k_mlp_mfma<<<CTOT * YMLP, 256, 0, stream>>>(x_h, x_l, W1P, W2P, mb1, mb2,
```

Measured after the change: 679.0 us. 35.5% more time.
